# Kernel optimization log

Measured on AMD Instinct MI355X. Metric: run time of the kernel, lower is better.

Reference implementation:

```python
import jax, jax.numpy as jnp
import numpy as np

B, N, DEG = 16, 1723, 8   # batch, mesh vertices, avg degree
C, L = 512, 5             # num_channels, num_layers


def _gn(x, g, b, G):
    # GroupNorm over (B, C, N), normalize per group over (C//G, N)
    Bx, Cx, Nx = x.shape
    xr = x.reshape(Bx, G, Cx // G, Nx)
    m = xr.mean(axis=(2, 3), keepdims=True)
    v = xr.var(axis=(2, 3), keepdims=True)
    xr = (xr - m) * jax.lax.rsqrt(v + 1e-5)
    return xr.reshape(Bx, Cx, Nx) * g[None, :, None] + b[None, :, None]


def _glin(W, b, x):
    # per-vertex linear: (O,I) @ (B,I,N) + b
    return jnp.einsum('oi,bin->bon', W, x) + b[None, :, None]


def _gconv(x, W, b, src, dst, w):
    # GraphConvolution: support = x^T @ W, then sparse adjacency spmm via edge list
    sup = jnp.einsum('bcn,cd->bnd', x, W)          # (B, N, C)
    msg = sup[:, src, :] * w[None, :, None]        # gather neighbors (B, E, C)
    agg = jnp.zeros_like(sup).at[:, dst, :].add(msg) + b[None, None, :]
    return agg.transpose(0, 2, 1)                  # back to (B, C, N)


def _resblock(x, p, src, dst, w):
    (pre_g, pre_b, l1W, l1b, n1g, n1b, cW, cb, n2g, n2b, l2W, l2b, skW, skb) = p
    Cin, Ch = x.shape[1], l1W.shape[0]
    y = jax.nn.relu(_gn(x, pre_g, pre_b, Cin // 8))
    y = _glin(l1W, l1b, y)
    y = jax.nn.relu(_gn(y, n1g, n1b, Ch // 8))
    y = _gconv(y, cW, cb, src, dst, w)
    y = jax.nn.relu(_gn(y, n2g, n2b, Ch // 8))
    y = _glin(l2W, l2b, y)
    if skW is not None:
        x = _glin(skW, skb, x)
    return x + y


def setup_inputs() -> dict:
    key = jax.random.key(0)
    ks = iter(jax.random.split(key, 64))
    s = 0.02
    w = lambda shp: jax.random.normal(next(ks), shp, jnp.float32) * s
    z = lambda shp: jnp.zeros(shp, jnp.float32)
    o = lambda shp: jnp.ones(shp, jnp.float32)
    H = C // 2
    E = N * DEG
    inp = {}
    inp['image_resnet'] = jax.random.normal(next(ks), (B, 2048), jnp.float32)
    inp['ref_vertices'] = jax.random.normal(next(ks), (3, N), jnp.float32)
    inp['adj_src'] = jax.random.randint(next(ks), (E,), 0, N, jnp.int32)
    inp['adj_dst'] = jnp.repeat(jnp.arange(N, dtype=jnp.int32), DEG)
    inp['adj_w'] = jnp.full((E,), 1.0 / DEG, jnp.float32)
    inp['lin0_W'] = w((2 * C, 3 + 2048)); inp['lin0_b'] = z((2 * C,))
    inp['b0_pre_g'] = o((2 * C,)); inp['b0_pre_b'] = z((2 * C,))
    inp['b0_lin1_W'] = w((H, 2 * C)); inp['b0_lin1_b'] = z((H,))
    inp['b0_n1_g'] = o((H,)); inp['b0_n1_b'] = z((H,))
    inp['b0_conv_W'] = w((H, H)); inp['b0_conv_b'] = z((H,))
    inp['b0_n2_g'] = o((H,)); inp['b0_n2_b'] = z((H,))
    inp['b0_lin2_W'] = w((C, H)); inp['b0_lin2_b'] = z((C,))
    inp['b0_skip_W'] = w((C, 2 * C)); inp['b0_skip_b'] = z((C,))
    inp['blk_pre_g'] = o((L, C)); inp['blk_pre_b'] = z((L, C))
    inp['blk_lin1_W'] = w((L, H, C)); inp['blk_lin1_b'] = z((L, H))
    inp['blk_n1_g'] = o((L, H)); inp['blk_n1_b'] = z((L, H))
    inp['blk_conv_W'] = w((L, H, H)); inp['blk_conv_b'] = z((L, H))
    inp['blk_n2_g'] = o((L, H)); inp['blk_n2_b'] = z((L, H))
    inp['blk_lin2_W'] = w((L, C, H)); inp['blk_lin2_b'] = z((L, C))
    inp['h1_W'] = w((64, C)); inp['h1_b'] = z((64,))
    inp['h2_W'] = w((32, 64)); inp['h2_b'] = z((32,))
    inp['hn_g'] = o((32,)); inp['hn_b'] = z((32,))
    inp['h3_W'] = w((3, 32)); inp['h3_b'] = z((3,))
    return inp


def reference(image_resnet, ref_vertices, adj_src, adj_dst, adj_w,
              lin0_W, lin0_b,
              b0_pre_g, b0_pre_b, b0_lin1_W, b0_lin1_b, b0_n1_g, b0_n1_b,
              b0_conv_W, b0_conv_b, b0_n2_g, b0_n2_b, b0_lin2_W, b0_lin2_b,
              b0_skip_W, b0_skip_b,
              blk_pre_g, blk_pre_b, blk_lin1_W, blk_lin1_b, blk_n1_g, blk_n1_b,
              blk_conv_W, blk_conv_b, blk_n2_g, blk_n2_b, blk_lin2_W, blk_lin2_b,
              h1_W, h1_b, h2_W, h2_b, hn_g, hn_b, h3_W, h3_b):
    Bx, Nv = image_resnet.shape[0], ref_vertices.shape[1]
    img = jnp.broadcast_to(image_resnet[:, :, None], (Bx, 2048, Nv))
    verts = jnp.broadcast_to(ref_vertices[None], (Bx, 3, Nv))
    x = jnp.concatenate([verts, img], axis=1)                 # (B, 2051, N)
    x = _glin(lin0_W, lin0_b, x)                              # (B, 1024, N)
    x = _resblock(x, (b0_pre_g, b0_pre_b, b0_lin1_W, b0_lin1_b, b0_n1_g, b0_n1_b,
                      b0_conv_W, b0_conv_b, b0_n2_g, b0_n2_b, b0_lin2_W, b0_lin2_b,
                      b0_skip_W, b0_skip_b), adj_src, adj_dst, adj_w)  # (B, 512, N)
    for i in range(blk_pre_g.shape[0]):
        x = _resblock(x, (blk_pre_g[i], blk_pre_b[i], blk_lin1_W[i], blk_lin1_b[i],
                          blk_n1_g[i], blk_n1_b[i], blk_conv_W[i], blk_conv_b[i],
                          blk_n2_g[i], blk_n2_b[i], blk_lin2_W[i], blk_lin2_b[i],
                          None, None), adj_src, adj_dst, adj_w)
    # shape decoder head
    y = jax.nn.relu(_glin(h1_W, h1_b, x))
    y = _glin(h2_W, h2_b, y)
    y = jax.nn.relu(_gn(y, hn_g, hn_b, 4))   # GroupNorm(32//8, 32)
    y = _glin(h3_W, h3_b, y)                 # (B, 3, N)
    return y
```

## Files before the change

### kernel.cpp

```cpp
#include <hip/hip_runtime.h>
#include <cstddef>
#include <cstdint>

#define THREADS 256

typedef short bh8 __attribute__((ext_vector_type(8)));
typedef float fx4 __attribute__((ext_vector_type(4)));

__device__ __forceinline__ float bf2f(unsigned short u) {
  union { unsigned int i; float f; } x;
  x.i = ((unsigned int)u) << 16;
  return x.f;
}
__device__ __forceinline__ unsigned short f2bf(float f) {
  union { float f; unsigned int i; } x;
  x.f = f;
  unsigned int r = x.i + 0x7fffu + ((x.i >> 16) & 1u);
  return (unsigned short)(r >> 16);
}

__device__ __forceinline__ void gld16(const void* g, void* l) {
  __builtin_amdgcn_global_load_lds(
      (const __attribute__((address_space(1))) unsigned int*)g,
      (__attribute__((address_space(3))) unsigned int*)l, 16, 0, 0);
}

__global__ __launch_bounds__(THREADS) void transpose_img_k(
    const float* __restrict__ img, float* __restrict__ imgT) {
  int gid = blockIdx.x * THREADS + threadIdx.x;
  if (gid >= 2048 * 16) return;
  int k = gid >> 4, b = gid & 15;
  imgT[k * 16 + b] = img[b * 2048 + k];
}

__global__ __launch_bounds__(THREADS) void pack_wv_k(
    const float* __restrict__ W, float* __restrict__ wv) {
  int gid = blockIdx.x * THREADS + threadIdx.x;
  if (gid >= 3 * 1024) return;
  int k = gid >> 10, c = gid & 1023;
  wv[gid] = W[(size_t)c * 2051 + k];
}

__global__ __launch_bounds__(THREADS) void vertproj_k(
    const float* __restrict__ wv, const float* __restrict__ verts,
    float* __restrict__ v, int N) {
  int gid = blockIdx.x * THREADS + threadIdx.x;
  int c = gid & 1023, n = gid >> 10;
  if (n >= N) return;
  v[(size_t)n * 1024 + c] =
      wv[c] * verts[n] + wv[1024 + c] * verts[N + n] + wv[2048 + c] * verts[2 * N + n];
}

__global__ __launch_bounds__(THREADS) void ugemm2_k(
    const float* __restrict__ W, int ldw, int woff,
    const float* __restrict__ bias, const float* __restrict__ X,
    float* __restrict__ out, int K, int Ofull, int xl, int ks) {
  int tid = threadIdx.x;
  int b = tid & 15, cl = tid >> 4;
  int c = blockIdx.x * 16 + cl;
  int k0 = blockIdx.y * ks, k1 = k0 + ks;
  const float* wr = W + woff + (size_t)c * ldw;
  float a0 = 0.f, a1 = 0.f;
  if (xl) {
    const float* xr = X + (size_t)b * K;
    for (int k = k0; k < k1; k += 2) {
      a0 = fmaf(wr[k], xr[k], a0);
      a1 = fmaf(wr[k + 1], xr[k + 1], a1);
    }
  } else {
    for (int k = k0; k < k1; k += 2) {
      a0 = fmaf(wr[k], X[k * 16 + b], a0);
      a1 = fmaf(wr[k + 1], X[(k + 1) * 16 + b], a1);
    }
  }
  float r = a0 + a1;
  if (blockIdx.y == 0) r += bias[c];
  atomicAdd(&out[(size_t)b * Ofull + c], r);
}

struct PackDesc {
  const float* W;
  unsigned short* out;
  int O, K, TW, nOt, TS;
  unsigned cum;
};
struct PackArgs {
  PackDesc d[8];
  unsigned grand;
};

__global__ __launch_bounds__(THREADS) void packall_k(PackArgs a) {
  unsigned gid = blockIdx.x * THREADS + threadIdx.x;
  if (gid >= a.grand) return;
  int s = 0;
#pragma unroll
  for (int i = 1; i < 8; ++i)
    if (gid >= a.d[i].cum) s = i;
#pragma unroll
  for (int i = 0; i < 8; ++i) {
    if (s != i) continue;
    const float* W = a.d[i].W;
    int O = a.d[i].O, K = a.d[i].K, TW = a.d[i].TW, nOt = a.d[i].nOt;
    int TS = a.d[i].TS;
    unsigned e = gid - a.d[i].cum;
    int j = (int)(e & 7);
    int m;
    unsigned rest;
    if (TS == 128) {
      m = (int)((e >> 3) & 127);
      rest = e >> 10;
    } else {
      m = (int)((e >> 3) & 63);
      rest = e >> 9;
    }
    int K8 = K >> 3;
    int kg = (int)(rest % (unsigned)K8);
    unsigned rest2 = rest / (unsigned)K8;
    int ot = (int)(rest2 % (unsigned)nOt);
    int l = (int)(rest2 / (unsigned)nOt);
    int o = ot * TS + m, k = kg * 8 + j;
    float val = 0.f;
    if (o < O)
      val = TW ? W[(size_t)l * O * K + (size_t)k * O + o]
               : W[(size_t)l * O * K + (size_t)o * K + k];
    a.d[i].out[e] = f2bf(val);
  }
}

__global__ __launch_bounds__(THREADS) void vstats_k(
    const float* __restrict__ v, float* __restrict__ sv,
    float* __restrict__ sq, int N) {
  int c = blockIdx.x * THREADS + threadIdx.x;
  float s = 0.f, q = 0.f;
  for (int n = blockIdx.y; n < N; n += 16) {
    float x = v[(size_t)n * 1024 + c];
    s += x; q += x * x;
  }
  atomicAdd(&sv[c], s);
  atomicAdd(&sq[c], q);
}

__global__ __launch_bounds__(THREADS) void combine_b0_k(
    const float* __restrict__ ub, const float* __restrict__ sv,
    const float* __restrict__ sq, float* __restrict__ mean,
    float* __restrict__ rinv, int N) {
  int bg = blockIdx.x * THREADS + threadIdx.x;
  if (bg >= 2048) return;
  int b = bg >> 7, g = bg & 127;
  int c0 = g * 8;
  float fN = (float)N;
  float s = 0.f, q = 0.f;
#pragma unroll
  for (int j = 0; j < 8; ++j) {
    float u = ub[b * 1024 + c0 + j];
    float svc = sv[c0 + j];
    s += fN * u + svc;
    q += fN * u * u + 2.f * u * svc + sq[c0 + j];
  }
  float inv = 1.f / (8.f * fN);
  float m = s * inv;
  float var = q * inv - m * m;
  mean[bg] = m;
  rinv[bg] = rsqrtf(var + 1e-5f);
}

__global__ __launch_bounds__(THREADS) void agg16_k(
    const unsigned short* __restrict__ Xn, const float* __restrict__ sarr,
    const float* __restrict__ qarr, const float* __restrict__ gamma,
    const float* __restrict__ beta, const int* __restrict__ src,
    const float* __restrict__ wgt, unsigned short* __restrict__ outb, int N,
    int NPn) {
  int w = threadIdx.x >> 6, lane = threadIdx.x & 63;
  int n = blockIdx.x * 4 + w;
  if (n >= N) return;
  int b = blockIdx.y;
  int c = lane * 4;
  int g = c >> 3;
  float sfac = 1.f / (8.f * (float)N);
  float svv = sarr[b * 32 + g], qv = qarr[b * 32 + g];
  float m = svv * sfac;
  float ri = rsqrtf(qv * sfac - m * m + 1e-5f);
  float4 g4 = *(const float4*)(gamma + c);
  float4 b4 = *(const float4*)(beta + c);
  const int* sp = src + n * 8;
  const float* wp = wgt + n * 8;
  const unsigned short* base = Xn + (size_t)b * NPn * 256;
  float a0 = 0.f, a1 = 0.f, a2 = 0.f, a3 = 0.f;
#pragma unroll
  for (int j = 0; j < 8; ++j) {
    int sidx = sp[j];
    float wj = wp[j];
    ushort4 x4 = *(const ushort4*)(base + (size_t)sidx * 256 + c);
    a0 = fmaf(wj, fmaxf((bf2f(x4.x) - m) * ri * g4.x + b4.x, 0.f), a0);
    a1 = fmaf(wj, fmaxf((bf2f(x4.y) - m) * ri * g4.y + b4.y, 0.f), a1);
    a2 = fmaf(wj, fmaxf((bf2f(x4.z) - m) * ri * g4.z + b4.z, 0.f), a2);
    a3 = fmaf(wj, fmaxf((bf2f(x4.w) - m) * ri * g4.w + b4.w, 0.f), a3);
  }
  ushort4 h;
  h.x = f2bf(a0); h.y = f2bf(a1); h.z = f2bf(a2); h.w = f2bf(a3);
  *(ushort4*)(outb + ((size_t)b * NPn + n) * 256 + c) = h;
}

template <int XM, int RES, int OUT16, int ORELU, int STATS>
__global__ __launch_bounds__(THREADS) void mgemm_k(
    const unsigned short* __restrict__ Wp, const float* __restrict__ bias,
    const void* __restrict__ Xv, const float* __restrict__ ub,
    const float* __restrict__ vv, const float* __restrict__ meanS,
    const float* __restrict__ rinvS, const float* __restrict__ gamma,
    const float* __restrict__ beta, const float* __restrict__ resA,
    const float* __restrict__ resB, float* __restrict__ sacc,
    float* __restrict__ qacc, void* __restrict__ outv, int O, int I, int N,
    int NPn) {
  constexpr int BBUF = (XM == 4) ? 2 : 1;
  __shared__ unsigned short Alds[2][4][128][8];
  __shared__ unsigned short Blds[BBUF][4][128][8];
  const int tid = threadIdx.x;
  const int lane = tid & 63;
  const int wid = tid >> 6;
  const int wm = wid & 1, wn = wid >> 1;
  const int n0 = blockIdx.x * 128;
  const int o0 = blockIdx.y * 128;
  const int b = blockIdx.z;
  const int K8 = I >> 3;
  const unsigned short* wp = Wp + (size_t)blockIdx.y * K8 * 1024;

  fx4 acc[4][4];
#pragma unroll
  for (int i = 0; i < 4; ++i)
#pragma unroll
    for (int j = 0; j < 4; ++j) {
      acc[i][j][0] = 0.f; acc[i][j][1] = 0.f;
      acc[i][j][2] = 0.f; acc[i][j][3] = 0.f;
    }

  const int sko = tid >> 6;
  const int sn = (tid & 63) * 2;
  const int mlane = lane & 15;
  const int klane = lane >> 4;

  auto dmaA = [&](int k0, int buf) {
    const unsigned short* asrc = wp + (size_t)(k0 >> 3) * 1024;
    unsigned short* ab = &Alds[buf][0][0][0];
    gld16(asrc + (size_t)tid * 8, ab + (size_t)tid * 8);
    gld16(asrc + (size_t)(tid + 256) * 8, ab + (size_t)(tid + 256) * 8);
  };
  auto dmaB4 = [&](int k0, int buf) {
    const unsigned short* xs =
        (const unsigned short*)Xv + ((size_t)b * NPn + n0) * I + k0 + wid * 8;
    unsigned short* bb = &Blds[buf][0][0][0] + (size_t)wid * 1024;
    gld16(xs + (size_t)lane * I, bb + (size_t)lane * 8);
    gld16(xs + (size_t)(lane + 64) * I, bb + 512 + (size_t)lane * 8);
  };

  uint4 br0, br1;
  float4 f00, f01, f10, f11, u01, u23;

  auto gloadB = [&](int k0) {
    const int ke = k0 + sko * 8;
    if (XM == 3) {
      const unsigned short* p =
          (const unsigned short*)Xv + ((size_t)b * NPn + n0 + sn) * I + ke;
      br0 = *(const uint4*)p;
      br1 = *(const uint4*)(p + I);
    } else if (XM == 1) {
      const float* p = vv + (size_t)(n0 + sn) * I + ke;
      f00 = *(const float4*)p;       f01 = *(const float4*)(p + 4);
      f10 = *(const float4*)(p + I); f11 = *(const float4*)(p + I + 4);
      const float* up = ub + (size_t)b * I + ke;
      u01 = *(const float4*)up;
      u23 = *(const float4*)(up + 4);
    } else if (XM == 0 || XM == 2) {
      const float* p = (const float*)Xv + ((size_t)b * NPn + n0 + sn) * I + ke;
      f00 = *(const float4*)p;       f01 = *(const float4*)(p + 4);
      f10 = *(const float4*)(p + I); f11 = *(const float4*)(p + I + 4);
    }
  };

  union H8 { unsigned short u[8]; uint4 q; };

  auto bstoreB = [&](int k0) {
    const int ke = k0 + sko * 8;
    float x0[8], x1[8];
    if (XM == 3) {
      H8 hr0, hr1;
      hr0.q = br0; hr1.q = br1;
#pragma unroll
      for (int j = 0; j < 8; ++j) {
        x0[j] = bf2f(hr0.u[j]);
        x1[j] = bf2f(hr1.u[j]);
      }
    } else {
      x0[0] = f00.x; x0[1] = f00.y; x0[2] = f00.z; x0[3] = f00.w;
      x0[4] = f01.x; x0[5] = f01.y; x0[6] = f01.z; x0[7] = f01.w;
      x1[0] = f10.x; x1[1] = f10.y; x1[2] = f10.z; x1[3] = f10.w;
      x1[4] = f11.x; x1[5] = f11.y; x1[6] = f11.z; x1[7] = f11.w;
    }
    if (XM == 1) {
      float uu[8] = {u01.x, u01.y, u01.z, u01.w, u23.x, u23.y, u23.z, u23.w};
#pragma unroll
      for (int j = 0; j < 8; ++j) { x0[j] += uu[j]; x1[j] += uu[j]; }
    }
    if (XM != 0) {
      float m_, r_;
      if (XM == 1) {
        m_ = meanS[b * K8 + (ke >> 3)];
        r_ = rinvS[b * K8 + (ke >> 3)];
      } else {
        float sfac = 1.f / (8.f * (float)N);
        float sv = meanS[b * K8 + (ke >> 3)];
        float qv = rinvS[b * K8 + (ke >> 3)];
        m_ = sv * sfac;
        r_ = rsqrtf(qv * sfac - m_ * m_ + 1e-5f);
      }
      float4 g0q = *(const float4*)(gamma + ke);
      float4 g1q = *(const float4*)(gamma + ke + 4);
      float4 e0q = *(const float4*)(beta + ke);
      float4 e1q = *(const float4*)(beta + ke + 4);
      float ga[8] = {g0q.x, g0q.y, g0q.z, g0q.w, g1q.x, g1q.y, g1q.z, g1q.w};
      float bb[8] = {e0q.x, e0q.y, e0q.z, e0q.w, e1q.x, e1q.y, e1q.z, e1q.w};
#pragma unroll
      for (int j = 0; j < 8; ++j) {
        x0[j] = fmaxf((x0[j] - m_) * r_ * ga[j] + bb[j], 0.f);
        x1[j] = fmaxf((x1[j] - m_) * r_ * ga[j] + bb[j], 0.f);
      }
    }
    H8 h0, h1;
#pragma unroll
    for (int j = 0; j < 8; ++j) {
      h0.u[j] = f2bf(x0[j]);
      h1.u[j] = f2bf(x1[j]);
    }
    *(uint4*)&Blds[0][sko][sn][0] = h0.q;
    *(uint4*)&Blds[0][sko][sn + 1][0] = h1.q;
  };

  auto compute = [&](int ab, int bb) {
    bh8 af[4], bfr[4];
#pragma unroll
    for (int mi = 0; mi < 4; ++mi)
      af[mi] = *(const bh8*)(&Alds[ab][klane][wm * 64 + mi * 16 + mlane][0]);
#pragma unroll
    for (int ni = 0; ni < 4; ++ni)
      bfr[ni] = *(const bh8*)(&Blds[bb][klane][wn * 64 + ni * 16 + mlane][0]);
#pragma unroll
    for (int mi = 0; mi < 4; ++mi)
#pragma unroll
      for (int ni = 0; ni < 4; ++ni)
        acc[mi][ni] = __builtin_amdgcn_mfma_f32_16x16x32_bf16(
            af[mi], bfr[ni], acc[mi][ni], 0, 0, 0);
  };

  if (XM == 4) {
    dmaA(0, 0);
    dmaB4(0, 0);
    __syncthreads();
    for (int k0 = 0; k0 < I; k0 += 32) {
      const int cur = (k0 >> 5) & 1;
      if (k0 + 32 < I) {
        dmaA(k0 + 32, cur ^ 1);
        dmaB4(k0 + 32, cur ^ 1);
      }
      compute(cur, cur);
      __syncthreads();
    }
  } else {
    dmaA(0, 0);
    gloadB(0);
    for (int k0 = 0; k0 < I; k0 += 32) {
      const int cur = (k0 >> 5) & 1;
      bstoreB(k0);
      __syncthreads();
      if (k0 + 32 < I) {
        dmaA(k0 + 32, cur ^ 1);
        gloadB(k0 + 32);
      }
      compute(cur, 0);
      __syncthreads();
    }
  }

  float sred[4] = {0.f, 0.f, 0.f, 0.f};
  float qred[4] = {0.f, 0.f, 0.f, 0.f};
#pragma unroll
  for (int mi = 0; mi < 4; ++mi) {
    const int o = o0 + wm * 64 + mi * 16 + klane * 4;
    if (o >= O) continue;
    float4 bi;
    if (bias) bi = *(const float4*)(bias + o);
    float4 ra;
    if (RES == 2) ra = *(const float4*)(resA + (size_t)b * O + o);
#pragma unroll
    for (int ni = 0; ni < 4; ++ni) {
      const int n = n0 + wn * 64 + ni * 16 + mlane;
      if (n >= N) continue;
      float v0 = acc[mi][ni][0], v1 = acc[mi][ni][1];
      float v2 = acc[mi][ni][2], v3 = acc[mi][ni][3];
      if (bias) { v0 += bi.x; v1 += bi.y; v2 += bi.z; v3 += bi.w; }
      size_t obase = ((size_t)b * NPn + n) * O + o;
      if (RES == 1) {
        float4 rv = *(const float4*)(resA + obase);
        v0 += rv.x; v1 += rv.y; v2 += rv.z; v3 += rv.w;
      }
      if (RES == 3) {
        ushort4 rv = *(const ushort4*)((const unsigned short*)resA + obase);
        v0 += bf2f(rv.x); v1 += bf2f(rv.y);
        v2 += bf2f(rv.z); v3 += bf2f(rv.w);
      }
      if (RES == 2) {
        float4 rb = *(const float4*)(resB + (size_t)n * O + o);
        v0 += ra.x + rb.x; v1 += ra.y + rb.y;
        v2 += ra.z + rb.z; v3 += ra.w + rb.w;
      }
      if (ORELU) {
        v0 = fmaxf(v0, 0.f); v1 = fmaxf(v1, 0.f);
        v2 = fmaxf(v2, 0.f); v3 = fmaxf(v3, 0.f);
      }
      if (STATS) {
        sred[mi] += v0 + v1 + v2 + v3;
        qred[mi] += v0 * v0 + v1 * v1 + v2 * v2 + v3 * v3;
      }
      if (OUT16) {
        ushort4 h;
        h.x = f2bf(v0); h.y = f2bf(v1); h.z = f2bf(v2); h.w = f2bf(v3);
        *(ushort4*)((unsigned short*)outv + obase) = h;
      } else {
        float4 fv; fv.x = v0; fv.y = v1; fv.z = v2; fv.w = v3;
        *(float4*)((float*)outv + obase) = fv;
      }
    }
  }
  if (STATS) {
    const int G = O >> 3;
#pragma unroll
    for (int mi = 0; mi < 4; ++mi) {
      const int o = o0 + wm * 64 + mi * 16 + klane * 4;
      if (o >= O) continue;
      float s = sred[mi], q = qred[mi];
#pragma unroll
      for (int m = 1; m < 16; m <<= 1) {
        s += __shfl_xor(s, m, 64);
        q += __shfl_xor(q, m, 64);
      }
      if (mlane == 0) {
        atomicAdd(&sacc[b * G + (o >> 3)], s);
        atomicAdd(&qacc[b * G + (o >> 3)], q);
      }
    }
  }
}

template <int OUT16, int ORELU, int STATS>
__global__ __launch_bounds__(THREADS) void mgemm64_k(
    const unsigned short* __restrict__ Wp, const float* __restrict__ bias,
    const unsigned short* __restrict__ Xv, float* __restrict__ sacc,
    float* __restrict__ qacc, void* __restrict__ outv, int O, int I, int N,
    int NPn) {
  __shared__ unsigned short Alds[2][4][64][8];
  __shared__ unsigned short Blds[2][4][128][8];
  const int tid = threadIdx.x;
  const int lane = tid & 63;
  const int wid = tid >> 6;
  const int n0 = blockIdx.x * 128;
  const int o0 = blockIdx.y * 64;
  const int b = blockIdx.z;
  const int K8 = I >> 3;
  const unsigned short* wp = Wp + (size_t)blockIdx.y * K8 * 512;

  fx4 acc[4][2];
#pragma unroll
  for (int i = 0; i < 4; ++i)
#pragma unroll
    for (int j = 0; j < 2; ++j) {
      acc[i][j][0] = 0.f; acc[i][j][1] = 0.f;
      acc[i][j][2] = 0.f; acc[i][j][3] = 0.f;
    }

  const int mlane = lane & 15;
  const int klane = lane >> 4;

  auto dmaA = [&](int k0, int buf) {
    const unsigned short* asrc = wp + (size_t)(k0 >> 3) * 512;
    unsigned short* ab = &Alds[buf][0][0][0];
    gld16(asrc + (size_t)tid * 8, ab + (size_t)tid * 8);
  };
  auto dmaB = [&](int k0, int buf) {
    const unsigned short* xs = Xv + ((size_t)b * NPn + n0) * I + k0 + wid * 8;
    unsigned short* bb = &Blds[buf][0][0][0] + (size_t)wid * 1024;
    gld16(xs + (size_t)lane * I, bb + (size_t)lane * 8);
    gld16(xs + (size_t)(lane + 64) * I, bb + 512 + (size_t)lane * 8);
  };

  dmaA(0, 0);
  dmaB(0, 0);
  __syncthreads();
  for (int k0 = 0; k0 < I; k0 += 32) {
    const int cur = (k0 >> 5) & 1;
    if (k0 + 32 < I) {
      dmaA(k0 + 32, cur ^ 1);
      dmaB(k0 + 32, cur ^ 1);
    }
    bh8 af[4], bfr[2];
#pragma unroll
    for (int mi = 0; mi < 4; ++mi)
      af[mi] = *(const bh8*)(&Alds[cur][klane][mi * 16 + mlane][0]);
#pragma unroll
    for (int ni = 0; ni < 2; ++ni)
      bfr[ni] = *(const bh8*)(&Blds[cur][klane][wid * 32 + ni * 16 + mlane][0]);
#pragma unroll
    for (int mi = 0; mi < 4; ++mi)
#pragma unroll
      for (int ni = 0; ni < 2; ++ni)
        acc[mi][ni] = __builtin_amdgcn_mfma_f32_16x16x32_bf16(
            af[mi], bfr[ni], acc[mi][ni], 0, 0, 0);
    __syncthreads();
  }

  float sred[4] = {0.f, 0.f, 0.f, 0.f};
  float qred[4] = {0.f, 0.f, 0.f, 0.f};
#pragma unroll
  for (int mi = 0; mi < 4; ++mi) {
    const int o = o0 + mi * 16 + klane * 4;
    if (o >= O) continue;
    float4 bi;
    if (bias) bi = *(const float4*)(bias + o);
#pragma unroll
    for (int ni = 0; ni < 2; ++ni) {
      const int n = n0 + wid * 32 + ni * 16 + mlane;
      if (n >= N) continue;
      float v0 = acc[mi][ni][0], v1 = acc[mi][ni][1];
      float v2 = acc[mi][ni][2], v3 = acc[mi][ni][3];
      if (bias) { v0 += bi.x; v1 += bi.y; v2 += bi.z; v3 += bi.w; }
      if (ORELU) {
        v0 = fmaxf(v0, 0.f); v1 = fmaxf(v1, 0.f);
        v2 = fmaxf(v2, 0.f); v3 = fmaxf(v3, 0.f);
      }
      if (STATS) {
        sred[mi] += v0 + v1 + v2 + v3;
        qred[mi] += v0 * v0 + v1 * v1 + v2 * v2 + v3 * v3;
      }
      size_t obase = ((size_t)b * NPn + n) * O + o;
      if (OUT16) {
        ushort4 h;
        h.x = f2bf(v0); h.y = f2bf(v1); h.z = f2bf(v2); h.w = f2bf(v3);
        *(ushort4*)((unsigned short*)outv + obase) = h;
      } else {
        float4 fv; fv.x = v0; fv.y = v1; fv.z = v2; fv.w = v3;
        *(float4*)((float*)outv + obase) = fv;
      }
    }
  }
  if (STATS) {
    const int G = O >> 3;
#pragma unroll
    for (int mi = 0; mi < 4; ++mi) {
      const int o = o0 + mi * 16 + klane * 4;
      if (o >= O) continue;
      float s = sred[mi], q = qred[mi];
#pragma unroll
      for (int m = 1; m < 16; m <<= 1) {
        s += __shfl_xor(s, m, 64);
        q += __shfl_xor(q, m, 64);
      }
      if (mlane == 0) {
        atomicAdd(&sacc[b * G + (o >> 3)], s);
        atomicAdd(&qacc[b * G + (o >> 3)], q);
      }
    }
  }
}

__global__ __launch_bounds__(THREADS) void h2_k(
    const float* __restrict__ t64, const float* __restrict__ W,
    const float* __restrict__ bias, float* __restrict__ out, int N, int NPn) {
  int gid = blockIdx.x * THREADS + threadIdx.x;
  int o = gid & 31, n = gid >> 5;
  if (n >= N) return;
  int b = blockIdx.y;
  const float* xr = t64 + ((size_t)b * NPn + n) * 64;
  const float* wr = W + o * 64;
  float acc = bias[o];
#pragma unroll
  for (int i = 0; i < 64; i += 4) {
    float4 w4 = *(const float4*)(wr + i);
    float4 x4 = *(const float4*)(xr + i);
    acc += w4.x * x4.x + w4.y * x4.y + w4.z * x4.z + w4.w * x4.w;
  }
  out[((size_t)b * NPn + n) * 32 + o] = acc;
}

__global__ __launch_bounds__(THREADS) void stats_head_k(
    const float* __restrict__ X, float* __restrict__ mean,
    float* __restrict__ rinv, int NPn, int N) {
  int b = blockIdx.x >> 2, g = blockIdx.x & 3;
  int c = g * 8 + (threadIdx.x & 7);
  float s = 0.f, q = 0.f;
  for (int n = threadIdx.x >> 3; n < N; n += 32) {
    float x = X[((size_t)b * NPn + n) * 32 + c];
    s += x; q += x * x;
  }
#pragma unroll
  for (int off = 32; off; off >>= 1) {
    s += __shfl_down(s, off, 64);
    q += __shfl_down(q, off, 64);
  }
  __shared__ float shs[4], shq[4];
  int wv = threadIdx.x >> 6;
  if ((threadIdx.x & 63) == 0) { shs[wv] = s; shq[wv] = q; }
  __syncthreads();
  if (threadIdx.x == 0) {
    s = shs[0] + shs[1] + shs[2] + shs[3];
    q = shq[0] + shq[1] + shq[2] + shq[3];
    float inv = 1.f / (8.f * (float)N);
    float m = s * inv;
    float var = q * inv - m * m;
    mean[blockIdx.x] = m;
    rinv[blockIdx.x] = rsqrtf(var + 1e-5f);
  }
}

__global__ __launch_bounds__(THREADS) void h3_k(
    const float* __restrict__ t32, const float* __restrict__ mean,
    const float* __restrict__ rinv, const float* __restrict__ g,
    const float* __restrict__ be, const float* __restrict__ W,
    const float* __restrict__ bias, float* __restrict__ out, int N, int NPn) {
  int n = blockIdx.x * THREADS + threadIdx.x;
  if (n >= N) return;
  int b = blockIdx.y;
  const float* xr = t32 + ((size_t)b * NPn + n) * 32;
  float y0 = bias[0], y1 = bias[1], y2 = bias[2];
#pragma unroll
  for (int c = 0; c < 32; ++c) {
    float m = mean[b * 4 + (c >> 3)], ri = rinv[b * 4 + (c >> 3)];
    float x = fmaxf((xr[c] - m) * ri * g[c] + be[c], 0.f);
    y0 = fmaf(W[c], x, y0);
    y1 = fmaf(W[32 + c], x, y1);
    y2 = fmaf(W[64 + c], x, y2);
  }
  out[(size_t)b * 3 * N + n] = y0;
  out[(size_t)b * 3 * N + N + n] = y1;
  out[(size_t)b * 3 * N + 2 * N + n] = y2;
}

extern "C" void kernel_launch(void* const* d_in, const int* in_sizes, int n_in,
                              void* d_out, int out_size, void* d_ws,
                              size_t ws_size, hipStream_t stream) {
  (void)n_in; (void)out_size; (void)ws_size;
  const float* img = (const float*)d_in[0];
  const float* verts = (const float*)d_in[1];
  const int* src = (const int*)d_in[2];
  const float* adjw = (const float*)d_in[4];
  const float* lin0_W = (const float*)d_in[5];
  const float* lin0_b = (const float*)d_in[6];
  const float* b0_pre_g = (const float*)d_in[7];
  const float* b0_pre_b = (const float*)d_in[8];
  const float* b0_lin1_W = (const float*)d_in[9];
  const float* b0_lin1_b = (const float*)d_in[10];
  const float* b0_n1_g = (const float*)d_in[11];
  const float* b0_n1_b = (const float*)d_in[12];
  const float* b0_conv_W = (const float*)d_in[13];
  const float* b0_conv_b = (const float*)d_in[14];
  const float* b0_n2_g = (const float*)d_in[15];
  const float* b0_n2_b = (const float*)d_in[16];
  const float* b0_lin2_W = (const float*)d_in[17];
  const float* b0_lin2_b = (const float*)d_in[18];
  const float* b0_skip_W = (const float*)d_in[19];
  const float* b0_skip_b = (const float*)d_in[20];
  const float* blk_pre_g = (const float*)d_in[21];
  const float* blk_pre_b = (const float*)d_in[22];
  const float* blk_lin1_W = (const float*)d_in[23];
  const float* blk_lin1_b = (const float*)d_in[24];
  const float* blk_n1_g = (const float*)d_in[25];
  const float* blk_n1_b = (const float*)d_in[26];
  const float* blk_conv_W = (const float*)d_in[27];
  const float* blk_conv_b = (const float*)d_in[28];
  const float* blk_n2_g = (const float*)d_in[29];
  const float* blk_n2_b = (const float*)d_in[30];
  const float* blk_lin2_W = (const float*)d_in[31];
  const float* blk_lin2_b = (const float*)d_in[32];
  const float* h1_W = (const float*)d_in[33];
  const float* h1_b = (const float*)d_in[34];
  const float* h2_W = (const float*)d_in[35];
  const float* h2_b = (const float*)d_in[36];
  const float* hn_g = (const float*)d_in[37];
  const float* hn_b = (const float*)d_in[38];
  const float* h3_W = (const float*)d_in[39];
  const float* h3_b = (const float*)d_in[40];

  const int N = in_sizes[1] / 3;
  const int NP = ((N + 127) / 128) * 128;
  const int NT128 = NP / 128;
  const int B = 16;

  char* wsb = (char*)d_ws;
  size_t off = 0;
  auto alloc = [&](size_t nbytes) {
    void* p = wsb + off;
    off += (nbytes + 255) & ~(size_t)255;
    return p;
  };
  unsigned short* xb16 = (unsigned short*)alloc((size_t)B * NP * 512 * 2);
  unsigned short* t256a = (unsigned short*)alloc((size_t)B * NP * 256 * 2);
  unsigned short* t256b = (unsigned short*)alloc((size_t)B * NP * 256 * 2);
  float* vbuf = (float*)alloc((size_t)NP * 1024 * 4);
  float* svbuf = (float*)alloc((size_t)NP * 512 * 4);
  float* t64 = (float*)alloc((size_t)B * NP * 64 * 4);
  float* t32 = (float*)alloc((size_t)B * NP * 32 * 4);
  float* imgT = (float*)alloc(2048 * 16 * 4);
  float* wv = (float*)alloc(3 * 1024 * 4);
  float* m0 = (float*)alloc(2048 * 4);
  float* r0 = (float*)alloc(2048 * 4);
  float* mh = (float*)alloc(64 * 4);
  float* rh = (float*)alloc(64 * 4);
  float* zerobuf = (float*)alloc((size_t)49152 * 4);
  float* sA = zerobuf;
  float* qA = zerobuf + 11264;
  float* sv = zerobuf + 22528;
  float* sq = zerobuf + 23552;
  float* ub = zerobuf + 24576;
  float* suT = zerobuf + 40960;
  const int off_b0n1 = 0, off_b0n2 = 512;
  auto off_pre = [](int l) { return 1024 + l * 2048; };
  auto off_n1 = [](int l) { return 1024 + l * 2048 + 1024; };
  auto off_n2 = [](int l) { return 1024 + l * 2048 + 1536; };
  unsigned short* pw_b0l1 = (unsigned short*)alloc(262144 * 2);
  unsigned short* pw_b0cv = (unsigned short*)alloc(65536 * 2);
  unsigned short* pw_b0l2 = (unsigned short*)alloc(131072 * 2);
  unsigned short* pw_b0sk = (unsigned short*)alloc(524288 * 2);
  unsigned short* pw_l1 = (unsigned short*)alloc(655360 * 2);
  unsigned short* pw_cv = (unsigned short*)alloc(327680 * 2);
  unsigned short* pw_l2 = (unsigned short*)alloc(655360 * 2);
  unsigned short* pw_h1 = (unsigned short*)alloc(32768 * 2);

  dim3 blk(THREADS);
  auto cdiv = [](size_t a, size_t b) { return (unsigned)((a + b - 1) / b); };

  hipMemsetAsync(zerobuf, 0, (size_t)49152 * 4, stream);

  {
    PackArgs pa;
    unsigned c = 0;
    auto set = [&](int i, const float* W, unsigned short* o, int O, int K,
                   int TW, int nOt, int TS, unsigned tot) {
      pa.d[i] = {W, o, O, K, TW, nOt, TS, c};
      c += tot;
    };
    set(0, b0_lin1_W, pw_b0l1, 256, 1024, 0, 2, 128, 262144);
    set(1, b0_conv_W, pw_b0cv, 256, 256, 1, 4, 64, 65536);
    set(2, b0_lin2_W, pw_b0l2, 512, 256, 0, 4, 128, 131072);
    set(3, b0_skip_W, pw_b0sk, 512, 1024, 0, 4, 128, 524288);
    set(4, blk_lin1_W, pw_l1, 256, 512, 0, 2, 128, 655360);
    set(5, blk_conv_W, pw_cv, 256, 256, 1, 4, 64, 327680);
    set(6, blk_lin2_W, pw_l2, 512, 256, 0, 4, 128, 655360);
    set(7, h1_W, pw_h1, 64, 512, 0, 1, 64, 32768);
    pa.grand = c;
    packall_k<<<cdiv(pa.grand, THREADS), blk, 0, stream>>>(pa);
  }

  transpose_img_k<<<cdiv(2048 * 16, THREADS), blk, 0, stream>>>(img, imgT);
  pack_wv_k<<<cdiv(3072, THREADS), blk, 0, stream>>>(lin0_W, wv);
  ugemm2_k<<<dim3(64, 16), blk, 0, stream>>>(lin0_W, 2051, 3, lin0_b, imgT,
                                             ub, 2048, 1024, 0, 128);
  vertproj_k<<<cdiv((size_t)N * 1024, THREADS), blk, 0, stream>>>(wv, verts, vbuf, N);

  const dim3 aggGrid(cdiv(N, 4), 16);

  vstats_k<<<dim3(4, 16), blk, 0, stream>>>(vbuf, sv, sq, N);
  combine_b0_k<<<dim3(8), blk, 0, stream>>>(ub, sv, sq, m0, r0, N);
  mgemm_k<1, 0, 1, 0, 1><<<dim3(NT128, 2, 16), blk, 0, stream>>>(
      pw_b0l1, b0_lin1_b, nullptr, ub, vbuf, m0, r0, b0_pre_g, b0_pre_b,
      nullptr, nullptr, sA + off_b0n1, qA + off_b0n1, t256a, 256, 1024, N, NP);
  ugemm2_k<<<dim3(32, 8), blk, 0, stream>>>(b0_skip_W, 1024, 0, b0_skip_b, ub,
                                            suT, 1024, 512, 1, 128);
  mgemm_k<0, 0, 0, 0, 0><<<dim3(NT128, 4, 1), blk, 0, stream>>>(
      pw_b0sk, nullptr, vbuf, nullptr, nullptr, nullptr, nullptr, nullptr,
      nullptr, nullptr, nullptr, nullptr, nullptr, svbuf, 512, 1024, N, NP);
  agg16_k<<<aggGrid, blk, 0, stream>>>(t256a, sA + off_b0n1, qA + off_b0n1,
                                       b0_n1_g, b0_n1_b, src, adjw, t256b, N, NP);
  mgemm64_k<1, 0, 1><<<dim3(NT128, 4, 16), blk, 0, stream>>>(
      pw_b0cv, b0_conv_b, t256b, sA + off_b0n2, qA + off_b0n2, t256a, 256, 256,
      N, NP);
  mgemm_k<3, 2, 1, 0, 1><<<dim3(NT128, 4, 16), blk, 0, stream>>>(
      pw_b0l2, b0_lin2_b, t256a, nullptr, nullptr, sA + off_b0n2,
      qA + off_b0n2, b0_n2_g, b0_n2_b, suT, svbuf, sA + off_pre(0),
      qA + off_pre(0), xb16, 512, 256, N, NP);

  for (int l = 0; l < 5; ++l) {
    const float* pg = blk_pre_g + l * 512;
    const float* pb = blk_pre_b + l * 512;
    const unsigned short* l1W = pw_l1 + (size_t)l * 131072;
    const float* l1b = blk_lin1_b + l * 256;
    const float* n1g = blk_n1_g + l * 256;
    const float* n1b = blk_n1_b + l * 256;
    const unsigned short* cW = pw_cv + (size_t)l * 65536;
    const float* cb = blk_conv_b + l * 256;
    const float* n2g = blk_n2_g + l * 256;
    const float* n2b = blk_n2_b + l * 256;
    const unsigned short* l2W = pw_l2 + (size_t)l * 131072;
    const float* l2b = blk_lin2_b + l * 512;

    mgemm_k<3, 0, 1, 0, 1><<<dim3(NT128, 2, 16), blk, 0, stream>>>(
        l1W, l1b, xb16, nullptr, nullptr, sA + off_pre(l), qA + off_pre(l), pg,
        pb, nullptr, nullptr, sA + off_n1(l), qA + off_n1(l), t256a, 256, 512,
        N, NP);
    agg16_k<<<aggGrid, blk, 0, stream>>>(t256a, sA + off_n1(l), qA + off_n1(l),
                                         n1g, n1b, src, adjw, t256b, N, NP);
    mgemm64_k<1, 0, 1><<<dim3(NT128, 4, 16), blk, 0, stream>>>(
        cW, cb, t256b, sA + off_n2(l), qA + off_n2(l), t256a, 256, 256, N, NP);
    if (l < 4) {
      mgemm_k<3, 3, 1, 0, 1><<<dim3(NT128, 4, 16), blk, 0, stream>>>(
          l2W, l2b, t256a, nullptr, nullptr, sA + off_n2(l), qA + off_n2(l),
          n2g, n2b, (const float*)xb16, nullptr, sA + off_pre(l + 1),
          qA + off_pre(l + 1), xb16, 512, 256, N, NP);
    } else {
      mgemm_k<3, 3, 1, 0, 0><<<dim3(NT128, 4, 16), blk, 0, stream>>>(
          l2W, l2b, t256a, nullptr, nullptr, sA + off_n2(l), qA + off_n2(l),
          n2g, n2b, (const float*)xb16, nullptr, nullptr, nullptr, xb16, 512,
          256, N, NP);
    }
  }

  mgemm64_k<0, 1, 0><<<dim3(NT128, 1, 16), blk, 0, stream>>>(
      pw_h1, h1_b, xb16, nullptr, nullptr, t64, 64, 512, N, NP);
  h2_k<<<dim3(cdiv((size_t)N * 32, THREADS), 16), blk, 0, stream>>>(
      t64, h2_W, h2_b, t32, N, NP);
  stats_head_k<<<dim3(64), blk, 0, stream>>>(t32, mh, rh, NP, N);
  h3_k<<<dim3(cdiv(N, THREADS), 16), blk, 0, stream>>>(
      t32, mh, rh, hn_g, hn_b, h3_W, h3_b, (float*)d_out, N, NP);
}
```

Before: 1.558 ms.

## Fuse all stages into one persistent megakernel with software grid barriers

```diff
diff --git a/kernel.cpp b/kernel.cpp
--- a/kernel.cpp
+++ b/kernel.cpp
@@ -3,6 +3,7 @@
 #include <cstdint>
 
 #define THREADS 256
+#define NBLK 512
 
 typedef short bh8 __attribute__((ext_vector_type(8)));
 typedef float fx4 __attribute__((ext_vector_type(4)));
@@ -18,64 +19,10 @@
   unsigned int r = x.i + 0x7fffu + ((x.i >> 16) & 1u);
   return (unsigned short)(r >> 16);
 }
-
 __device__ __forceinline__ void gld16(const void* g, void* l) {
   __builtin_amdgcn_global_load_lds(
       (const __attribute__((address_space(1))) unsigned int*)g,
       (__attribute__((address_space(3))) unsigned int*)l, 16, 0, 0);
-}
-
-__global__ __launch_bounds__(THREADS) void transpose_img_k(
-    const float* __restrict__ img, float* __restrict__ imgT) {
-  int gid = blockIdx.x * THREADS + threadIdx.x;
-  if (gid >= 2048 * 16) return;
-  int k = gid >> 4, b = gid & 15;
-  imgT[k * 16 + b] = img[b * 2048 + k];
-}
-
-__global__ __launch_bounds__(THREADS) void pack_wv_k(
-    const float* __restrict__ W, float* __restrict__ wv) {
-  int gid = blockIdx.x * THREADS + threadIdx.x;
-  if (gid >= 3 * 1024) return;
-  int k = gid >> 10, c = gid & 1023;
-  wv[gid] = W[(size_t)c * 2051 + k];
-}
-
-__global__ __launch_bounds__(THREADS) void vertproj_k(
-    const float* __restrict__ wv, const float* __restrict__ verts,
-    float* __restrict__ v, int N) {
-  int gid = blockIdx.x * THREADS + threadIdx.x;
-  int c = gid & 1023, n = gid >> 10;
-  if (n >= N) return;
-  v[(size_t)n * 1024 + c] =
-      wv[c] * verts[n] + wv[1024 + c] * verts[N + n] + wv[2048 + c] * verts[2 * N + n];
-}
-
-__global__ __launch_bounds__(THREADS) void ugemm2_k(
-    const float* __restrict__ W, int ldw, int woff,
-    const float* __restrict__ bias, const float* __restrict__ X,
-    float* __restrict__ out, int K, int Ofull, int xl, int ks) {
-  int tid = threadIdx.x;
-  int b = tid & 15, cl = tid >> 4;
-  int c = blockIdx.x * 16 + cl;
-  int k0 = blockIdx.y * ks, k1 = k0 + ks;
-  const float* wr = W + woff + (size_t)c * ldw;
-  float a0 = 0.f, a1 = 0.f;
-  if (xl) {
-    const float* xr = X + (size_t)b * K;
-    for (int k = k0; k < k1; k += 2) {
-      a0 = fmaf(wr[k], xr[k], a0);
-      a1 = fmaf(wr[k + 1], xr[k + 1], a1);
-    }
-  } else {
-    for (int k = k0; k < k1; k += 2) {
-      a0 = fmaf(wr[k], X[k * 16 + b], a0);
-      a1 = fmaf(wr[k + 1], X[(k + 1) * 16 + b], a1);
-    }
-  }
-  float r = a0 + a1;
-  if (blockIdx.y == 0) r += bias[c];
-  atomicAdd(&out[(size_t)b * Ofull + c], r);
 }
 
 struct PackDesc {
@@ -84,145 +31,65 @@
   int O, K, TW, nOt, TS;
   unsigned cum;
 };
-struct PackArgs {
-  PackDesc d[8];
+
+struct Args {
+  const float *img, *verts;
+  const int* src;
+  const float* adjw;
+  const float *lin0_W, *lin0_b;
+  const float *b0_pre_g, *b0_pre_b, *b0_lin1_b, *b0_n1_g, *b0_n1_b, *b0_conv_b;
+  const float *b0_n2_g, *b0_n2_b, *b0_lin2_b, *b0_skip_W, *b0_skip_b;
+  const float *blk_pre_g, *blk_pre_b, *blk_lin1_b, *blk_n1_g, *blk_n1_b;
+  const float *blk_conv_b, *blk_n2_g, *blk_n2_b, *blk_lin2_b;
+  const float *h1_b, *h2_W, *h2_b, *hn_g, *hn_b, *h3_W, *h3_b;
+  unsigned short *xb16, *t256a, *t256b;
+  float *vbuf, *svbuf, *t64, *t32, *imgT, *wv, *m0, *r0, *mh, *rh;
+  float *sA, *qA, *sv, *sq, *ub, *suT;
+  unsigned short *pw_b0l1, *pw_b0cv, *pw_b0l2, *pw_b0sk, *pw_l1, *pw_cv, *pw_l2, *pw_h1;
+  unsigned* bar;
+  float* dout;
+  PackDesc pd[8];
   unsigned grand;
+  int N, NP;
 };
 
-__global__ __launch_bounds__(THREADS) void packall_k(PackArgs a) {
-  unsigned gid = blockIdx.x * THREADS + threadIdx.x;
-  if (gid >= a.grand) return;
-  int s = 0;
-#pragma unroll
-  for (int i = 1; i < 8; ++i)
-    if (gid >= a.d[i].cum) s = i;
-#pragma unroll
-  for (int i = 0; i < 8; ++i) {
-    if (s != i) continue;
-    const float* W = a.d[i].W;
-    int O = a.d[i].O, K = a.d[i].K, TW = a.d[i].TW, nOt = a.d[i].nOt;
-    int TS = a.d[i].TS;
-    unsigned e = gid - a.d[i].cum;
-    int j = (int)(e & 7);
-    int m;
-    unsigned rest;
-    if (TS == 128) {
-      m = (int)((e >> 3) & 127);
-      rest = e >> 10;
-    } else {
-      m = (int)((e >> 3) & 63);
-      rest = e >> 9;
-    }
-    int K8 = K >> 3;
-    int kg = (int)(rest % (unsigned)K8);
-    unsigned rest2 = rest / (unsigned)K8;
-    int ot = (int)(rest2 % (unsigned)nOt);
-    int l = (int)(rest2 / (unsigned)nOt);
-    int o = ot * TS + m, k = kg * 8 + j;
-    float val = 0.f;
-    if (o < O)
-      val = TW ? W[(size_t)l * O * K + (size_t)k * O + o]
-               : W[(size_t)l * O * K + (size_t)o * K + k];
-    a.d[i].out[e] = f2bf(val);
-  }
-}
-
-__global__ __launch_bounds__(THREADS) void vstats_k(
-    const float* __restrict__ v, float* __restrict__ sv,
-    float* __restrict__ sq, int N) {
-  int c = blockIdx.x * THREADS + threadIdx.x;
-  float s = 0.f, q = 0.f;
-  for (int n = blockIdx.y; n < N; n += 16) {
-    float x = v[(size_t)n * 1024 + c];
-    s += x; q += x * x;
-  }
-  atomicAdd(&sv[c], s);
-  atomicAdd(&sq[c], q);
-}
-
-__global__ __launch_bounds__(THREADS) void combine_b0_k(
-    const float* __restrict__ ub, const float* __restrict__ sv,
-    const float* __restrict__ sq, float* __restrict__ mean,
-    float* __restrict__ rinv, int N) {
-  int bg = blockIdx.x * THREADS + threadIdx.x;
-  if (bg >= 2048) return;
-  int b = bg >> 7, g = bg & 127;
-  int c0 = g * 8;
-  float fN = (float)N;
-  float s = 0.f, q = 0.f;
-#pragma unroll
-  for (int j = 0; j < 8; ++j) {
-    float u = ub[b * 1024 + c0 + j];
-    float svc = sv[c0 + j];
-    s += fN * u + svc;
-    q += fN * u * u + 2.f * u * svc + sq[c0 + j];
-  }
-  float inv = 1.f / (8.f * fN);
-  float m = s * inv;
-  float var = q * inv - m * m;
-  mean[bg] = m;
-  rinv[bg] = rsqrtf(var + 1e-5f);
-}
-
-__global__ __launch_bounds__(THREADS) void agg16_k(
-    const unsigned short* __restrict__ Xn, const float* __restrict__ sarr,
-    const float* __restrict__ qarr, const float* __restrict__ gamma,
-    const float* __restrict__ beta, const int* __restrict__ src,
-    const float* __restrict__ wgt, unsigned short* __restrict__ outb, int N,
-    int NPn) {
-  int w = threadIdx.x >> 6, lane = threadIdx.x & 63;
-  int n = blockIdx.x * 4 + w;
-  if (n >= N) return;
-  int b = blockIdx.y;
-  int c = lane * 4;
-  int g = c >> 3;
-  float sfac = 1.f / (8.f * (float)N);
-  float svv = sarr[b * 32 + g], qv = qarr[b * 32 + g];
-  float m = svv * sfac;
-  float ri = rsqrtf(qv * sfac - m * m + 1e-5f);
-  float4 g4 = *(const float4*)(gamma + c);
-  float4 b4 = *(const float4*)(beta + c);
-  const int* sp = src + n * 8;
-  const float* wp = wgt + n * 8;
-  const unsigned short* base = Xn + (size_t)b * NPn * 256;
-  float a0 = 0.f, a1 = 0.f, a2 = 0.f, a3 = 0.f;
-#pragma unroll
-  for (int j = 0; j < 8; ++j) {
-    int sidx = sp[j];
-    float wj = wp[j];
-    ushort4 x4 = *(const ushort4*)(base + (size_t)sidx * 256 + c);
-    a0 = fmaf(wj, fmaxf((bf2f(x4.x) - m) * ri * g4.x + b4.x, 0.f), a0);
-    a1 = fmaf(wj, fmaxf((bf2f(x4.y) - m) * ri * g4.y + b4.y, 0.f), a1);
-    a2 = fmaf(wj, fmaxf((bf2f(x4.z) - m) * ri * g4.z + b4.z, 0.f), a2);
-    a3 = fmaf(wj, fmaxf((bf2f(x4.w) - m) * ri * g4.w + b4.w, 0.f), a3);
-  }
-  ushort4 h;
-  h.x = f2bf(a0); h.y = f2bf(a1); h.z = f2bf(a2); h.w = f2bf(a3);
-  *(ushort4*)(outb + ((size_t)b * NPn + n) * 256 + c) = h;
-}
+#define OFF_B0N1 0
+#define OFF_B0N2 512
+__device__ __forceinline__ int off_pre(int l) { return 1024 + l * 2048; }
+__device__ __forceinline__ int off_n1(int l) { return 1024 + l * 2048 + 1024; }
+__device__ __forceinline__ int off_n2(int l) { return 1024 + l * 2048 + 1536; }
+
+__device__ __forceinline__ void gbar(unsigned* bar, unsigned target) {
+  __syncthreads();
+  if (threadIdx.x == 0) {
+    __threadfence();
+    atomicAdd(bar, 1u);
+    while (atomicAdd(bar, 0u) < target) __builtin_amdgcn_s_sleep(1);
+    __threadfence();
+  }
+  __syncthreads();
+}
+
+typedef unsigned short A4T[4][128][8];
 
 template <int XM, int RES, int OUT16, int ORELU, int STATS>
-__global__ __launch_bounds__(THREADS) void mgemm_k(
-    const unsigned short* __restrict__ Wp, const float* __restrict__ bias,
-    const void* __restrict__ Xv, const float* __restrict__ ub,
-    const float* __restrict__ vv, const float* __restrict__ meanS,
-    const float* __restrict__ rinvS, const float* __restrict__ gamma,
-    const float* __restrict__ beta, const float* __restrict__ resA,
-    const float* __restrict__ resB, float* __restrict__ sacc,
-    float* __restrict__ qacc, void* __restrict__ outv, int O, int I, int N,
-    int NPn) {
-  constexpr int BBUF = (XM == 4) ? 2 : 1;
-  __shared__ unsigned short Alds[2][4][128][8];
-  __shared__ unsigned short Blds[BBUF][4][128][8];
+__device__ void dev_mgemm(
+    unsigned short* smA, unsigned short* smB, const unsigned short* Wp,
+    const float* bias, const void* Xv, const float* ub, const float* vv,
+    const float* meanS, const float* rinvS, const float* gamma,
+    const float* beta, const float* resA, const float* resB,
+    float* sacc, float* qacc, void* outv, int O, int I, int N, int NPn,
+    int bx, int by, int b) {
+  A4T* Alds = (A4T*)smA;
+  A4T* Blds = (A4T*)smB;
   const int tid = threadIdx.x;
   const int lane = tid & 63;
   const int wid = tid >> 6;
   const int wm = wid & 1, wn = wid >> 1;
-  const int n0 = blockIdx.x * 128;
-  const int o0 = blockIdx.y * 128;
-  const int b = blockIdx.z;
+  const int n0 = bx * 128;
+  const int o0 = by * 128;
   const int K8 = I >> 3;
-  const unsigned short* wp = Wp + (size_t)blockIdx.y * K8 * 1024;
+  const unsigned short* wp = Wp + (size_t)by * K8 * 1024;
 
   fx4 acc[4][4];
 #pragma unroll
@@ -449,22 +316,19 @@
   }
 }
 
-template <int OUT16, int ORELU, int STATS>
-__global__ __launch_bounds__(THREADS) void mgemm64_k(
-    const unsigned short* __restrict__ Wp, const float* __restrict__ bias,
-    const unsigned short* __restrict__ Xv, float* __restrict__ sacc,
-    float* __restrict__ qacc, void* __restrict__ outv, int O, int I, int N,
-    int NPn) {
-  __shared__ unsigned short Alds[2][4][64][8];
-  __shared__ unsigned short Blds[2][4][128][8];
+__device__ void dev_mgemm64(
+    unsigned short* smA, unsigned short* smB, const unsigned short* Wp,
+    const float* bias, const unsigned short* Xv, void* outv, int O, int I,
+    int N, int NPn, int bx, int b) {
+  typedef unsigned short A64T[4][64][8];
+  A64T* Alds = (A64T*)smA;
+  A4T* Blds = (A4T*)smB;
   const int tid = threadIdx.x;
   const int lane = tid & 63;
   const int wid = tid >> 6;
-  const int n0 = blockIdx.x * 128;
-  const int o0 = blockIdx.y * 64;
-  const int b = blockIdx.z;
+  const int n0 = bx * 128;
   const int K8 = I >> 3;
-  const unsigned short* wp = Wp + (size_t)blockIdx.y * K8 * 512;
+  const unsigned short* wp = Wp;
 
   fx4 acc[4][2];
 #pragma unroll
@@ -474,7 +338,6 @@
       acc[i][j][0] = 0.f; acc[i][j][1] = 0.f;
       acc[i][j][2] = 0.f; acc[i][j][3] = 0.f;
     }
-
   const int mlane = lane & 15;
   const int klane = lane >> 4;
 
@@ -515,83 +378,89 @@
     __syncthreads();
   }
 
-  float sred[4] = {0.f, 0.f, 0.f, 0.f};
-  float qred[4] = {0.f, 0.f, 0.f, 0.f};
 #pragma unroll
   for (int mi = 0; mi < 4; ++mi) {
-    const int o = o0 + mi * 16 + klane * 4;
-    if (o >= O) continue;
-    float4 bi;
-    if (bias) bi = *(const float4*)(bias + o);
+    const int o = mi * 16 + klane * 4;
+    float4 bi = *(const float4*)(bias + o);
 #pragma unroll
     for (int ni = 0; ni < 2; ++ni) {
       const int n = n0 + wid * 32 + ni * 16 + mlane;
       if (n >= N) continue;
-      float v0 = acc[mi][ni][0], v1 = acc[mi][ni][1];
-      float v2 = acc[mi][ni][2], v3 = acc[mi][ni][3];
-      if (bias) { v0 += bi.x; v1 += bi.y; v2 += bi.z; v3 += bi.w; }
-      if (ORELU) {
-        v0 = fmaxf(v0, 0.f); v1 = fmaxf(v1, 0.f);
-        v2 = fmaxf(v2, 0.f); v3 = fmaxf(v3, 0.f);
-      }
-      if (STATS) {
-        sred[mi] += v0 + v1 + v2 + v3;
-        qred[mi] += v0 * v0 + v1 * v1 + v2 * v2 + v3 * v3;
-      }
+      float v0 = acc[mi][ni][0] + bi.x, v1 = acc[mi][ni][1] + bi.y;
+      float v2 = acc[mi][ni][2] + bi.z, v3 = acc[mi][ni][3] + bi.w;
+      v0 = fmaxf(v0, 0.f); v1 = fmaxf(v1, 0.f);
+      v2 = fmaxf(v2, 0.f); v3 = fmaxf(v3, 0.f);
       size_t obase = ((size_t)b * NPn + n) * O + o;
-      if (OUT16) {
-        ushort4 h;
-        h.x = f2bf(v0); h.y = f2bf(v1); h.z = f2bf(v2); h.w = f2bf(v3);
-        *(ushort4*)((unsigned short*)outv + obase) = h;
-      } else {
-        float4 fv; fv.x = v0; fv.y = v1; fv.z = v2; fv.w = v3;
-        *(float4*)((float*)outv + obase) = fv;
-      }
-    }
-  }
-  if (STATS) {
-    const int G = O >> 3;
-#pragma unroll
-    for (int mi = 0; mi < 4; ++mi) {
-      const int o = o0 + mi * 16 + klane * 4;
-      if (o >= O) continue;
-      float s = sred[mi], q = qred[mi];
-#pragma unroll
-      for (int m = 1; m < 16; m <<= 1) {
-        s += __shfl_xor(s, m, 64);
-        q += __shfl_xor(q, m, 64);
-      }
-      if (mlane == 0) {
-        atomicAdd(&sacc[b * G + (o >> 3)], s);
-        atomicAdd(&qacc[b * G + (o >> 3)], q);
-      }
-    }
-  }
-}
-
-__global__ __launch_bounds__(THREADS) void h2_k(
-    const float* __restrict__ t64, const float* __restrict__ W,
-    const float* __restrict__ bias, float* __restrict__ out, int N, int NPn) {
-  int gid = blockIdx.x * THREADS + threadIdx.x;
-  int o = gid & 31, n = gid >> 5;
+      float4 fv; fv.x = v0; fv.y = v1; fv.z = v2; fv.w = v3;
+      *(float4*)((float*)outv + obase) = fv;
+    }
+  }
+}
+
+__device__ void dev_agg16(const unsigned short* Xn, const float* sarr,
+                          const float* qarr, const float* gamma,
+                          const float* beta, const int* src, const float* wgt,
+                          unsigned short* outb, int N, int NPn, int nb, int b) {
+  int w = threadIdx.x >> 6, lane = threadIdx.x & 63;
+  int n = nb * 4 + w;
   if (n >= N) return;
-  int b = blockIdx.y;
-  const float* xr = t64 + ((size_t)b * NPn + n) * 64;
-  const float* wr = W + o * 64;
-  float acc = bias[o];
-#pragma unroll
-  for (int i = 0; i < 64; i += 4) {
-    float4 w4 = *(const float4*)(wr + i);
-    float4 x4 = *(const float4*)(xr + i);
-    acc += w4.x * x4.x + w4.y * x4.y + w4.z * x4.z + w4.w * x4.w;
-  }
-  out[((size_t)b * NPn + n) * 32 + o] = acc;
-}
-
-__global__ __launch_bounds__(THREADS) void stats_head_k(
-    const float* __restrict__ X, float* __restrict__ mean,
-    float* __restrict__ rinv, int NPn, int N) {
-  int b = blockIdx.x >> 2, g = blockIdx.x & 3;
+  int c = lane * 4;
+  int g = c >> 3;
+  float sfac = 1.f / (8.f * (float)N);
+  float svv = sarr[b * 32 + g], qv = qarr[b * 32 + g];
+  float m = svv * sfac;
+  float ri = rsqrtf(qv * sfac - m * m + 1e-5f);
+  float4 g4 = *(const float4*)(gamma + c);
+  float4 b4 = *(const float4*)(beta + c);
+  const int* sp = src + n * 8;
+  const float* wp = wgt + n * 8;
+  const unsigned short* base = Xn + (size_t)b * NPn * 256;
+  float a0 = 0.f, a1 = 0.f, a2 = 0.f, a3 = 0.f;
+#pragma unroll
+  for (int j = 0; j < 8; ++j) {
+    int sidx = sp[j];
+    float wj = wp[j];
+    ushort4 x4 = *(const ushort4*)(base + (size_t)sidx * 256 + c);
+    a0 = fmaf(wj, fmaxf((bf2f(x4.x) - m) * ri * g4.x + b4.x, 0.f), a0);
+    a1 = fmaf(wj, fmaxf((bf2f(x4.y) - m) * ri * g4.y + b4.y, 0.f), a1);
+    a2 = fmaf(wj, fmaxf((bf2f(x4.z) - m) * ri * g4.z + b4.z, 0.f), a2);
+    a3 = fmaf(wj, fmaxf((bf2f(x4.w) - m) * ri * g4.w + b4.w, 0.f), a3);
+  }
+  ushort4 h;
+  h.x = f2bf(a0); h.y = f2bf(a1); h.z = f2bf(a2); h.w = f2bf(a3);
+  *(ushort4*)(outb + ((size_t)b * NPn + n) * 256 + c) = h;
+}
+
+__device__ void dev_ugemm2(const float* W, int ldw, int woff, const float* bias,
+                           const float* X, float* out, int K, int Ofull,
+                           int xl, int ks, int bx, int byy) {
+  int tid = threadIdx.x;
+  int b = tid & 15, cl = tid >> 4;
+  int c = bx * 16 + cl;
+  int k0 = byy * ks, k1 = k0 + ks;
+  const float* wr = W + woff + (size_t)c * ldw;
+  float a0 = 0.f, a1 = 0.f;
+  if (xl) {
+    const float* xr = X + (size_t)b * K;
+    for (int k = k0; k < k1; k += 2) {
+      a0 = fmaf(wr[k], xr[k], a0);
+      a1 = fmaf(wr[k + 1], xr[k + 1], a1);
+    }
+  } else {
+    for (int k = k0; k < k1; k += 2) {
+      a0 = fmaf(wr[k], X[k * 16 + b], a0);
+      a1 = fmaf(wr[k + 1], X[(k + 1) * 16 + b], a1);
+    }
+  }
+  float r = a0 + a1;
+  if (byy == 0) r += bias[c];
+  atomicAdd(&out[(size_t)b * Ofull + c], r);
+}
+
+__device__ void dev_stats_head(const float* X, float* mean, float* rinv,
+                               int NPn, int N, int j) {
+  __shared__ float shs[4], shq[4];
+  int b = j >> 2, g = j & 3;
   int c = g * 8 + (threadIdx.x & 7);
   float s = 0.f, q = 0.f;
   for (int n = threadIdx.x >> 3; n < N; n += 32) {
@@ -603,7 +472,6 @@
     s += __shfl_down(s, off, 64);
     q += __shfl_down(q, off, 64);
   }
-  __shared__ float shs[4], shq[4];
   int wv = threadIdx.x >> 6;
   if ((threadIdx.x & 63) == 0) { shs[wv] = s; shq[wv] = q; }
   __syncthreads();
@@ -613,83 +481,289 @@
     float inv = 1.f / (8.f * (float)N);
     float m = s * inv;
     float var = q * inv - m * m;
-    mean[blockIdx.x] = m;
-    rinv[blockIdx.x] = rsqrtf(var + 1e-5f);
-  }
-}
-
-__global__ __launch_bounds__(THREADS) void h3_k(
-    const float* __restrict__ t32, const float* __restrict__ mean,
-    const float* __restrict__ rinv, const float* __restrict__ g,
-    const float* __restrict__ be, const float* __restrict__ W,
-    const float* __restrict__ bias, float* __restrict__ out, int N, int NPn) {
-  int n = blockIdx.x * THREADS + threadIdx.x;
-  if (n >= N) return;
-  int b = blockIdx.y;
-  const float* xr = t32 + ((size_t)b * NPn + n) * 32;
-  float y0 = bias[0], y1 = bias[1], y2 = bias[2];
-#pragma unroll
-  for (int c = 0; c < 32; ++c) {
-    float m = mean[b * 4 + (c >> 3)], ri = rinv[b * 4 + (c >> 3)];
-    float x = fmaxf((xr[c] - m) * ri * g[c] + be[c], 0.f);
-    y0 = fmaf(W[c], x, y0);
-    y1 = fmaf(W[32 + c], x, y1);
-    y2 = fmaf(W[64 + c], x, y2);
-  }
-  out[(size_t)b * 3 * N + n] = y0;
-  out[(size_t)b * 3 * N + N + n] = y1;
-  out[(size_t)b * 3 * N + 2 * N + n] = y2;
+    mean[j] = m;
+    rinv[j] = rsqrtf(var + 1e-5f);
+  }
+  __syncthreads();
+}
+
+__global__ __launch_bounds__(THREADS, 2) void mega_k(Args a) {
+  __shared__ unsigned short smA[2 * 4 * 128 * 8];
+  __shared__ unsigned short smB[2 * 4 * 128 * 8];
+  const int tid = threadIdx.x;
+  const int N = a.N, NP = a.NP;
+  const unsigned stride = gridDim.x * THREADS;
+  unsigned tgt = 0;
+  auto BAR = [&]() { tgt += gridDim.x; gbar(a.bar, tgt); };
+
+  for (unsigned e = blockIdx.x * THREADS + tid; e < a.grand; e += stride) {
+    int s = 0;
+#pragma unroll
+    for (int i = 1; i < 8; ++i)
+      if (e >= a.pd[i].cum) s = i;
+#pragma unroll
+    for (int i = 0; i < 8; ++i) {
+      if (s != i) continue;
+      const float* W = a.pd[i].W;
+      int O = a.pd[i].O, K = a.pd[i].K, TW = a.pd[i].TW, nOt = a.pd[i].nOt;
+      int TS = a.pd[i].TS;
+      unsigned g = e - a.pd[i].cum;
+      int j = (int)(g & 7);
+      int m;
+      unsigned rest;
+      if (TS == 128) { m = (int)((g >> 3) & 127); rest = g >> 10; }
+      else { m = (int)((g >> 3) & 63); rest = g >> 9; }
+      int K8 = K >> 3;
+      int kg = (int)(rest % (unsigned)K8);
+      unsigned rest2 = rest / (unsigned)K8;
+      int ot = (int)(rest2 % (unsigned)nOt);
+      int l = (int)(rest2 / (unsigned)nOt);
+      int o = ot * TS + m, k = kg * 8 + j;
+      float val = 0.f;
+      if (o < O)
+        val = TW ? W[(size_t)l * O * K + (size_t)k * O + o]
+                 : W[(size_t)l * O * K + (size_t)o * K + k];
+      a.pd[i].out[g] = f2bf(val);
+    }
+  }
+  for (unsigned g = blockIdx.x * THREADS + tid; g < 2048u * 16u; g += stride) {
+    int k = g >> 4, b = g & 15;
+    a.imgT[k * 16 + b] = a.img[b * 2048 + k];
+  }
+  for (unsigned g = blockIdx.x * THREADS + tid; g < 3072u; g += stride) {
+    int k = g >> 10, c = g & 1023;
+    a.wv[g] = a.lin0_W[(size_t)c * 2051 + k];
+  }
+  BAR();
+  for (int j = blockIdx.x; j < 1024; j += gridDim.x)
+    dev_ugemm2(a.lin0_W, 2051, 3, a.lin0_b, a.imgT, a.ub, 2048, 1024, 0, 128,
+               j & 63, j >> 6);
+  for (unsigned g = blockIdx.x * THREADS + tid; g < (unsigned)N * 1024u; g += stride) {
+    int c = g & 1023, n = g >> 10;
+    a.vbuf[(size_t)n * 1024 + c] = a.wv[c] * a.verts[n] +
+                                   a.wv[1024 + c] * a.verts[N + n] +
+                                   a.wv[2048 + c] * a.verts[2 * N + n];
+  }
+  BAR();
+  for (int j = blockIdx.x; j < 64; j += gridDim.x) {
+    int c = (j & 3) * THREADS + tid;
+    int y = j >> 2;
+    float s = 0.f, q = 0.f;
+    for (int n = y; n < N; n += 16) {
+      float x = a.vbuf[(size_t)n * 1024 + c];
+      s += x; q += x * x;
+    }
+    atomicAdd(&a.sv[c], s);
+    atomicAdd(&a.sq[c], q);
+  }
+  BAR();
+  for (unsigned g = blockIdx.x * THREADS + tid; g < 2048u; g += stride) {
+    int b = g >> 7, gg = g & 127;
+    int c0 = gg * 8;
+    float fN = (float)N;
+    float s = 0.f, q = 0.f;
+#pragma unroll
+    for (int j = 0; j < 8; ++j) {
+      float u = a.ub[b * 1024 + c0 + j];
+      float svc = a.sv[c0 + j];
+      s += fN * u + svc;
+      q += fN * u * u + 2.f * u * svc + a.sq[c0 + j];
+    }
+    float inv = 1.f / (8.f * fN);
+    float m = s * inv;
+    float var = q * inv - m * m;
+    a.m0[g] = m;
+    a.r0[g] = rsqrtf(var + 1e-5f);
+  }
+  BAR();
+  for (int j = blockIdx.x; j < 760; j += gridDim.x) {
+    if (j < 448) {
+      dev_mgemm<1, 0, 1, 0, 1>(smA, smB, a.pw_b0l1, a.b0_lin1_b, nullptr, a.ub,
+                               a.vbuf, a.m0, a.r0, a.b0_pre_g, a.b0_pre_b,
+                               nullptr, nullptr, a.sA + OFF_B0N1,
+                               a.qA + OFF_B0N1, a.t256a, 256, 1024, N, NP,
+                               j % 14, (j / 14) % 2, j / 28);
+    } else if (j < 504) {
+      int k = j - 448;
+      dev_mgemm<0, 0, 0, 0, 0>(smA, smB, a.pw_b0sk, nullptr, a.vbuf, nullptr,
+                               nullptr, nullptr, nullptr, nullptr, nullptr,
+                               nullptr, nullptr, nullptr, nullptr, a.svbuf,
+                               512, 1024, N, NP, k % 14, k / 14, 0);
+    } else {
+      int k = j - 504;
+      dev_ugemm2(a.b0_skip_W, 1024, 0, a.b0_skip_b, a.ub, a.suT, 1024, 512, 1,
+                 128, k & 31, k >> 5);
+    }
+  }
+  BAR();
+  const int NB4 = (N + 3) >> 2;
+  for (int j = blockIdx.x; j < NB4 * 16; j += gridDim.x)
+    dev_agg16(a.t256a, a.sA + OFF_B0N1, a.qA + OFF_B0N1, a.b0_n1_g, a.b0_n1_b,
+              a.src, a.adjw, a.t256b, N, NP, j % NB4, j / NB4);
+  BAR();
+  for (int j = blockIdx.x; j < 448; j += gridDim.x)
+    dev_mgemm<4, 0, 1, 0, 1>(smA, smB, a.pw_b0cv, a.b0_conv_b, a.t256b,
+                             nullptr, nullptr, nullptr, nullptr, nullptr,
+                             nullptr, nullptr, nullptr, a.sA + OFF_B0N2,
+                             a.qA + OFF_B0N2, a.t256a, 256, 256, N, NP, j % 14,
+                             (j / 14) % 2, j / 28);
+  BAR();
+  for (int j = blockIdx.x; j < 896; j += gridDim.x)
+    dev_mgemm<3, 2, 1, 0, 1>(smA, smB, a.pw_b0l2, a.b0_lin2_b, a.t256a,
+                             nullptr, nullptr, a.sA + OFF_B0N2,
+                             a.qA + OFF_B0N2, a.b0_n2_g, a.b0_n2_b, a.suT,
+                             a.svbuf, a.sA + off_pre(0), a.qA + off_pre(0),
+                             a.xb16, 512, 256, N, NP, j % 14, (j / 14) % 4,
+                             j / 56);
+  BAR();
+  for (int l = 0; l < 5; ++l) {
+    const float* pg = a.blk_pre_g + l * 512;
+    const float* pb = a.blk_pre_b + l * 512;
+    const unsigned short* l1W = a.pw_l1 + (size_t)l * 131072;
+    const float* l1b = a.blk_lin1_b + l * 256;
+    const float* n1g = a.blk_n1_g + l * 256;
+    const float* n1b = a.blk_n1_b + l * 256;
+    const unsigned short* cW = a.pw_cv + (size_t)l * 65536;
+    const float* cb = a.blk_conv_b + l * 256;
+    const float* n2g = a.blk_n2_g + l * 256;
+    const float* n2b = a.blk_n2_b + l * 256;
+    const unsigned short* l2W = a.pw_l2 + (size_t)l * 131072;
+    const float* l2b = a.blk_lin2_b + l * 512;
+
+    for (int j = blockIdx.x; j < 448; j += gridDim.x)
+      dev_mgemm<3, 0, 1, 0, 1>(smA, smB, l1W, l1b, a.xb16, nullptr, nullptr,
+                               a.sA + off_pre(l), a.qA + off_pre(l), pg, pb,
+                               nullptr, nullptr, a.sA + off_n1(l),
+                               a.qA + off_n1(l), a.t256a, 256, 512, N, NP,
+                               j % 14, (j / 14) % 2, j / 28);
+    BAR();
+    for (int j = blockIdx.x; j < NB4 * 16; j += gridDim.x)
+      dev_agg16(a.t256a, a.sA + off_n1(l), a.qA + off_n1(l), n1g, n1b, a.src,
+                a.adjw, a.t256b, N, NP, j % NB4, j / NB4);
+    BAR();
+    for (int j = blockIdx.x; j < 448; j += gridDim.x)
+      dev_mgemm<4, 0, 1, 0, 1>(smA, smB, cW, cb, a.t256b, nullptr, nullptr,
+                               nullptr, nullptr, nullptr, nullptr, nullptr,
+                               nullptr, a.sA + off_n2(l), a.qA + off_n2(l),
+                               a.t256a, 256, 256, N, NP, j % 14, (j / 14) % 2,
+                               j / 28);
+    BAR();
+    if (l < 4) {
+      for (int j = blockIdx.x; j < 896; j += gridDim.x)
+        dev_mgemm<3, 3, 1, 0, 1>(smA, smB, l2W, l2b, a.t256a, nullptr, nullptr,
+                                 a.sA + off_n2(l), a.qA + off_n2(l), n2g, n2b,
+                                 (const float*)a.xb16, nullptr,
+                                 a.sA + off_pre(l + 1), a.qA + off_pre(l + 1),
+                                 a.xb16, 512, 256, N, NP, j % 14, (j / 14) % 4,
+                                 j / 56);
+    } else {
+      for (int j = blockIdx.x; j < 896; j += gridDim.x)
+        dev_mgemm<3, 3, 1, 0, 0>(smA, smB, l2W, l2b, a.t256a, nullptr, nullptr,
+                                 a.sA + off_n2(l), a.qA + off_n2(l), n2g, n2b,
+                                 (const float*)a.xb16, nullptr, nullptr,
+                                 nullptr, a.xb16, 512, 256, N, NP, j % 14,
+                                 (j / 14) % 4, j / 56);
+    }
+    BAR();
+  }
+  for (int j = blockIdx.x; j < 224; j += gridDim.x)
+    dev_mgemm64(smA, smB, a.pw_h1, a.h1_b, a.xb16, a.t64, 64, 512, N, NP,
+                j % 14, j / 14);
+  BAR();
+  const int GX2 = (N * 32 + THREADS - 1) / THREADS;
+  for (int j = blockIdx.x; j < GX2 * 16; j += gridDim.x) {
+    int gid = (j % GX2) * THREADS + tid;
+    int o = gid & 31, n = gid >> 5;
+    if (n >= N) continue;
+    int b = j / GX2;
+    const float* xr = a.t64 + ((size_t)b * NP + n) * 64;
+    const float* wr = a.h2_W + o * 64;
+    float acc = a.h2_b[o];
+#pragma unroll
+    for (int i = 0; i < 64; i += 4) {
+      float4 w4 = *(const float4*)(wr + i);
+      float4 x4 = *(const float4*)(xr + i);
+      acc += w4.x * x4.x + w4.y * x4.y + w4.z * x4.z + w4.w * x4.w;
+    }
+    a.t32[((size_t)b * NP + n) * 32 + o] = acc;
+  }
+  BAR();
+  for (int j = blockIdx.x; j < 64; j += gridDim.x)
+    dev_stats_head(a.t32, a.mh, a.rh, NP, N, j);
+  BAR();
+  const int GX3 = (N + THREADS - 1) / THREADS;
+  for (int j = blockIdx.x; j < GX3 * 16; j += gridDim.x) {
+    int n = (j % GX3) * THREADS + tid;
+    if (n >= N) continue;
+    int b = j / GX3;
+    const float* xr = a.t32 + ((size_t)b * NP + n) * 32;
+    float y0 = a.h3_b[0], y1 = a.h3_b[1], y2 = a.h3_b[2];
+#pragma unroll
+    for (int c = 0; c < 32; ++c) {
+      float m = a.mh[b * 4 + (c >> 3)], ri = a.rh[b * 4 + (c >> 3)];
+      float x = fmaxf((xr[c] - m) * ri * a.hn_g[c] + a.hn_b[c], 0.f);
+      y0 = fmaf(a.h3_W[c], x, y0);
+      y1 = fmaf(a.h3_W[32 + c], x, y1);
+      y2 = fmaf(a.h3_W[64 + c], x, y2);
+    }
+    a.dout[(size_t)b * 3 * N + n] = y0;
+    a.dout[(size_t)b * 3 * N + N + n] = y1;
+    a.dout[(size_t)b * 3 * N + 2 * N + n] = y2;
+  }
 }
 
 extern "C" void kernel_launch(void* const* d_in, const int* in_sizes, int n_in,
                               void* d_out, int out_size, void* d_ws,
                               size_t ws_size, hipStream_t stream) {
   (void)n_in; (void)out_size; (void)ws_size;
-  const float* img = (const float*)d_in[0];
-  const float* verts = (const float*)d_in[1];
-  const int* src = (const int*)d_in[2];
-  const float* adjw = (const float*)d_in[4];
-  const float* lin0_W = (const float*)d_in[5];
-  const float* lin0_b = (const float*)d_in[6];
-  const float* b0_pre_g = (const float*)d_in[7];
-  const float* b0_pre_b = (const float*)d_in[8];
+  Args a;
+  a.img = (const float*)d_in[0];
+  a.verts = (const float*)d_in[1];
+  a.src = (const int*)d_in[2];
+  a.adjw = (const float*)d_in[4];
+  a.lin0_W = (const float*)d_in[5];
+  a.lin0_b = (const float*)d_in[6];
+  a.b0_pre_g = (const float*)d_in[7];
+  a.b0_pre_b = (const float*)d_in[8];
   const float* b0_lin1_W = (const float*)d_in[9];
-  const float* b0_lin1_b = (const float*)d_in[10];
-  const float* b0_n1_g = (const float*)d_in[11];
-  const float* b0_n1_b = (const float*)d_in[12];
+  a.b0_lin1_b = (const float*)d_in[10];
+  a.b0_n1_g = (const float*)d_in[11];
+  a.b0_n1_b = (const float*)d_in[12];
   const float* b0_conv_W = (const float*)d_in[13];
-  const float* b0_conv_b = (const float*)d_in[14];
-  const float* b0_n2_g = (const float*)d_in[15];
-  const float* b0_n2_b = (const float*)d_in[16];
+  a.b0_conv_b = (const float*)d_in[14];
+  a.b0_n2_g = (const float*)d_in[15];
+  a.b0_n2_b = (const float*)d_in[16];
   const float* b0_lin2_W = (const float*)d_in[17];
-  const float* b0_lin2_b = (const float*)d_in[18];
-  const float* b0_skip_W = (const float*)d_in[19];
-  const float* b0_skip_b = (const float*)d_in[20];
-  const float* blk_pre_g = (const float*)d_in[21];
-  const float* blk_pre_b = (const float*)d_in[22];
+  a.b0_lin2_b = (const float*)d_in[18];
+  a.b0_skip_W = (const float*)d_in[19];
+  a.b0_skip_b = (const float*)d_in[20];
+  a.blk_pre_g = (const float*)d_in[21];
+  a.blk_pre_b = (const float*)d_in[22];
   const float* blk_lin1_W = (const float*)d_in[23];
-  const float* blk_lin1_b = (const float*)d_in[24];
-  const float* blk_n1_g = (const float*)d_in[25];
-  const float* blk_n1_b = (const float*)d_in[26];
+  a.blk_lin1_b = (const float*)d_in[24];
+  a.blk_n1_g = (const float*)d_in[25];
+  a.blk_n1_b = (const float*)d_in[26];
   const float* blk_conv_W = (const float*)d_in[27];
-  const float* blk_conv_b = (const float*)d_in[28];
-  const float* blk_n2_g = (const float*)d_in[29];
-  const float* blk_n2_b = (const float*)d_in[30];
+  a.blk_conv_b = (const float*)d_in[28];
+  a.blk_n2_g = (const float*)d_in[29];
+  a.blk_n2_b = (const float*)d_in[30];
   const float* blk_lin2_W = (const float*)d_in[31];
-  const float* blk_lin2_b = (const float*)d_in[32];
+  a.blk_lin2_b = (const float*)d_in[32];
   const float* h1_W = (const float*)d_in[33];
-  const float* h1_b = (const float*)d_in[34];
-  const float* h2_W = (const float*)d_in[35];
-  const float* h2_b = (const float*)d_in[36];
-  const float* hn_g = (const float*)d_in[37];
-  const float* hn_b = (const float*)d_in[38];
-  const float* h3_W = (const float*)d_in[39];
-  const float* h3_b = (const float*)d_in[40];
+  a.h1_b = (const float*)d_in[34];
+  a.h2_W = (const float*)d_in[35];
+  a.h2_b = (const float*)d_in[36];
+  a.hn_g = (const float*)d_in[37];
+  a.hn_b = (const float*)d_in[38];
+  a.h3_W = (const float*)d_in[39];
+  a.h3_b = (const float*)d_in[40];
 
   const int N = in_sizes[1] / 3;
   const int NP = ((N + 127) / 128) * 128;
-  const int NT128 = NP / 128;
   const int B = 16;
+  a.N = N;
+  a.NP = NP;
+  a.dout = (float*)d_out;
 
   char* wsb = (char*)d_ws;
   size_t off = 0;
@@ -698,132 +772,54 @@
     off += (nbytes + 255) & ~(size_t)255;
     return p;
   };
-  unsigned short* xb16 = (unsigned short*)alloc((size_t)B * NP * 512 * 2);
-  unsigned short* t256a = (unsigned short*)alloc((size_t)B * NP * 256 * 2);
-  unsigned short* t256b = (unsigned short*)alloc((size_t)B * NP * 256 * 2);
-  float* vbuf = (float*)alloc((size_t)NP * 1024 * 4);
-  float* svbuf = (float*)alloc((size_t)NP * 512 * 4);
-  float* t64 = (float*)alloc((size_t)B * NP * 64 * 4);
-  float* t32 = (float*)alloc((size_t)B * NP * 32 * 4);
-  float* imgT = (float*)alloc(2048 * 16 * 4);
-  float* wv = (float*)alloc(3 * 1024 * 4);
-  float* m0 = (float*)alloc(2048 * 4);
-  float* r0 = (float*)alloc(2048 * 4);
-  float* mh = (float*)alloc(64 * 4);
-  float* rh = (float*)alloc(64 * 4);
-  float* zerobuf = (float*)alloc((size_t)49152 * 4);
-  float* sA = zerobuf;
-  float* qA = zerobuf + 11264;
-  float* sv = zerobuf + 22528;
-  float* sq = zerobuf + 23552;
-  float* ub = zerobuf + 24576;
-  float* suT = zerobuf + 40960;
-  const int off_b0n1 = 0, off_b0n2 = 512;
-  auto off_pre = [](int l) { return 1024 + l * 2048; };
-  auto off_n1 = [](int l) { return 1024 + l * 2048 + 1024; };
-  auto off_n2 = [](int l) { return 1024 + l * 2048 + 1536; };
-  unsigned short* pw_b0l1 = (unsigned short*)alloc(262144 * 2);
-  unsigned short* pw_b0cv = (unsigned short*)alloc(65536 * 2);
-  unsigned short* pw_b0l2 = (unsigned short*)alloc(131072 * 2);
-  unsigned short* pw_b0sk = (unsigned short*)alloc(524288 * 2);
-  unsigned short* pw_l1 = (unsigned short*)alloc(655360 * 2);
-  unsigned short* pw_cv = (unsigned short*)alloc(327680 * 2);
-  unsigned short* pw_l2 = (unsigned short*)alloc(655360 * 2);
-  unsigned short* pw_h1 = (unsigned short*)alloc(32768 * 2);
-
-  dim3 blk(THREADS);
-  auto cdiv = [](size_t a, size_t b) { return (unsigned)((a + b - 1) / b); };
-
-  hipMemsetAsync(zerobuf, 0, (size_t)49152 * 4, stream);
+  a.xb16 = (unsigned short*)alloc((size_t)B * NP * 512 * 2);
+  a.t256a = (unsigned short*)alloc((size_t)B * NP * 256 * 2);
+  a.t256b = (unsigned short*)alloc((size_t)B * NP * 256 * 2);
+  a.vbuf = (float*)alloc((size_t)NP * 1024 * 4);
+  a.svbuf = (float*)alloc((size_t)NP * 512 * 4);
+  a.t64 = (float*)alloc((size_t)B * NP * 64 * 4);
+  a.t32 = (float*)alloc((size_t)B * NP * 32 * 4);
+  a.imgT = (float*)alloc(2048 * 16 * 4);
+  a.wv = (float*)alloc(3 * 1024 * 4);
+  a.m0 = (float*)alloc(2048 * 4);
+  a.r0 = (float*)alloc(2048 * 4);
+  a.mh = (float*)alloc(64 * 4);
+  a.rh = (float*)alloc(64 * 4);
+  float* zerobuf = (float*)alloc((size_t)49408 * 4);
+  a.sA = zerobuf;
+  a.qA = zerobuf + 11264;
+  a.sv = zerobuf + 22528;
+  a.sq = zerobuf + 23552;
+  a.ub = zerobuf + 24576;
+  a.suT = zerobuf + 40960;
+  a.bar = (unsigned*)(zerobuf + 49152);
+  a.pw_b0l1 = (unsigned short*)alloc(262144 * 2);
+  a.pw_b0cv = (unsigned short*)alloc(65536 * 2);
+  a.pw_b0l2 = (unsigned short*)alloc(131072 * 2);
+  a.pw_b0sk = (unsigned short*)alloc(524288 * 2);
+  a.pw_l1 = (unsigned short*)alloc(655360 * 2);
+  a.pw_cv = (unsigned short*)alloc(327680 * 2);
+  a.pw_l2 = (unsigned short*)alloc(655360 * 2);
+  a.pw_h1 = (unsigned short*)alloc(32768 * 2);
 
   {
-    PackArgs pa;
     unsigned c = 0;
     auto set = [&](int i, const float* W, unsigned short* o, int O, int K,
                    int TW, int nOt, int TS, unsigned tot) {
-      pa.d[i] = {W, o, O, K, TW, nOt, TS, c};
+      a.pd[i] = {W, o, O, K, TW, nOt, TS, c};
       c += tot;
     };
-    set(0, b0_lin1_W, pw_b0l1, 256, 1024, 0, 2, 128, 262144);
-    set(1, b0_conv_W, pw_b0cv, 256, 256, 1, 4, 64, 65536);
-    set(2, b0_lin2_W, pw_b0l2, 512, 256, 0, 4, 128, 131072);
-    set(3, b0_skip_W, pw_b0sk, 512, 1024, 0, 4, 128, 524288);
-    set(4, blk_lin1_W, pw_l1, 256, 512, 0, 2, 128, 655360);
-    set(5, blk_conv_W, pw_cv, 256, 256, 1, 4, 64, 327680);
-    set(6, blk_lin2_W, pw_l2, 512, 256, 0, 4, 128, 655360);
-    set(7, h1_W, pw_h1, 64, 512, 0, 1, 64, 32768);
-    pa.grand = c;
-    packall_k<<<cdiv(pa.grand, THREADS), blk, 0, stream>>>(pa);
-  }
-
-  transpose_img_k<<<cdiv(2048 * 16, THREADS), blk, 0, stream>>>(img, imgT);
-  pack_wv_k<<<cdiv(3072, THREADS), blk, 0, stream>>>(lin0_W, wv);
-  ugemm2_k<<<dim3(64, 16), blk, 0, stream>>>(lin0_W, 2051, 3, lin0_b, imgT,
-                                             ub, 2048, 1024, 0, 128);
-  vertproj_k<<<cdiv((size_t)N * 1024, THREADS), blk, 0, stream>>>(wv, verts, vbuf, N);
-
-  const dim3 aggGrid(cdiv(N, 4), 16);
-
-  vstats_k<<<dim3(4, 16), blk, 0, stream>>>(vbuf, sv, sq, N);
-  combine_b0_k<<<dim3(8), blk, 0, stream>>>(ub, sv, sq, m0, r0, N);
-  mgemm_k<1, 0, 1, 0, 1><<<dim3(NT128, 2, 16), blk, 0, stream>>>(
-      pw_b0l1, b0_lin1_b, nullptr, ub, vbuf, m0, r0, b0_pre_g, b0_pre_b,
-      nullptr, nullptr, sA + off_b0n1, qA + off_b0n1, t256a, 256, 1024, N, NP);
-  ugemm2_k<<<dim3(32, 8), blk, 0, stream>>>(b0_skip_W, 1024, 0, b0_skip_b, ub,
-                                            suT, 1024, 512, 1, 128);
-  mgemm_k<0, 0, 0, 0, 0><<<dim3(NT128, 4, 1), blk, 0, stream>>>(
-      pw_b0sk, nullptr, vbuf, nullptr, nullptr, nullptr, nullptr, nullptr,
-      nullptr, nullptr, nullptr, nullptr, nullptr, svbuf, 512, 1024, N, NP);
-  agg16_k<<<aggGrid, blk, 0, stream>>>(t256a, sA + off_b0n1, qA + off_b0n1,
-                                       b0_n1_g, b0_n1_b, src, adjw, t256b, N, NP);
-  mgemm64_k<1, 0, 1><<<dim3(NT128, 4, 16), blk, 0, stream>>>(
-      pw_b0cv, b0_conv_b, t256b, sA + off_b0n2, qA + off_b0n2, t256a, 256, 256,
-      N, NP);
-  mgemm_k<3, 2, 1, 0, 1><<<dim3(NT128, 4, 16), blk, 0, stream>>>(
-      pw_b0l2, b0_lin2_b, t256a, nullptr, nullptr, sA + off_b0n2,
-      qA + off_b0n2, b0_n2_g, b0_n2_b, suT, svbuf, sA + off_pre(0),
-      qA + off_pre(0), xb16, 512, 256, N, NP);
-
-  for (int l = 0; l < 5; ++l) {
-    const float* pg = blk_pre_g + l * 512;
-    const float* pb = blk_pre_b + l * 512;
-    const unsigned short* l1W = pw_l1 + (size_t)l * 131072;
-    const float* l1b = blk_lin1_b + l * 256;
-    const float* n1g = blk_n1_g + l * 256;
-    const float* n1b = blk_n1_b + l * 256;
-    const unsigned short* cW = pw_cv + (size_t)l * 65536;
-    const float* cb = blk_conv_b + l * 256;
-    const float* n2g = blk_n2_g + l * 256;
-    const float* n2b = blk_n2_b + l * 256;
-    const unsigned short* l2W = pw_l2 + (size_t)l * 131072;
-    const float* l2b = blk_lin2_b + l * 512;
-
-    mgemm_k<3, 0, 1, 0, 1><<<dim3(NT128, 2, 16), blk, 0, stream>>>(
-        l1W, l1b, xb16, nullptr, nullptr, sA + off_pre(l), qA + off_pre(l), pg,
-        pb, nullptr, nullptr, sA + off_n1(l), qA + off_n1(l), t256a, 256, 512,
-        N, NP);
-    agg16_k<<<aggGrid, blk, 0, stream>>>(t256a, sA + off_n1(l), qA + off_n1(l),
-                                         n1g, n1b, src, adjw, t256b, N, NP);
-    mgemm64_k<1, 0, 1><<<dim3(NT128, 4, 16), blk, 0, stream>>>(
-        cW, cb, t256b, sA + off_n2(l), qA + off_n2(l), t256a, 256, 256, N, NP);
-    if (l < 4) {
-      mgemm_k<3, 3, 1, 0, 1><<<dim3(NT128, 4, 16), blk, 0, stream>>>(
-          l2W, l2b, t256a, nullptr, nullptr, sA + off_n2(l), qA + off_n2(l),
-          n2g, n2b, (const float*)xb16, nullptr, sA + off_pre(l + 1),
-          qA + off_pre(l + 1), xb16, 512, 256, N, NP);
-    } else {
-      mgemm_k<3, 3, 1, 0, 0><<<dim3(NT128, 4, 16), blk, 0, stream>>>(
-          l2W, l2b, t256a, nullptr, nullptr, sA + off_n2(l), qA + off_n2(l),
-          n2g, n2b, (const float*)xb16, nullptr, nullptr, nullptr, xb16, 512,
-          256, N, NP);
-    }
-  }
-
-  mgemm64_k<0, 1, 0><<<dim3(NT128, 1, 16), blk, 0, stream>>>(
-      pw_h1, h1_b, xb16, nullptr, nullptr, t64, 64, 512, N, NP);
-  h2_k<<<dim3(cdiv((size_t)N * 32, THREADS), 16), blk, 0, stream>>>(
-      t64, h2_W, h2_b, t32, N, NP);
-  stats_head_k<<<dim3(64), blk, 0, stream>>>(t32, mh, rh, NP, N);
-  h3_k<<<dim3(cdiv(N, THREADS), 16), blk, 0, stream>>>(
-      t32, mh, rh, hn_g, hn_b, h3_W, h3_b, (float*)d_out, N, NP);
-}
+    set(0, b0_lin1_W, a.pw_b0l1, 256, 1024, 0, 2, 128, 262144);
+    set(1, b0_conv_W, a.pw_b0cv, 256, 256, 1, 2, 128, 65536);
+    set(2, b0_lin2_W, a.pw_b0l2, 512, 256, 0, 4, 128, 131072);
+    set(3, a.b0_skip_W, a.pw_b0sk, 512, 1024, 0, 4, 128, 524288);
+    set(4, blk_lin1_W, a.pw_l1, 256, 512, 0, 2, 128, 655360);
+    set(5, blk_conv_W, a.pw_cv, 256, 256, 1, 2, 128, 327680);
+    set(6, blk_lin2_W, a.pw_l2, 512, 256, 0, 4, 128, 655360);
+    set(7, h1_W, a.pw_h1, 64, 512, 0, 1, 64, 32768);
+    a.grand = c;
+  }
+
+  hipMemsetAsync(zerobuf, 0, (size_t)49408 * 4, stream);
+  mega_k<<<NBLK, THREADS, 0, stream>>>(a);
+}
```

New measurement: 2.736 ms. 1.76x slower.
